# Optimization experiments

Measured on AMD Instinct MI355X. Metric: run time of the kernel, lower is better.

Reference implementation:

```python
import jax, jax.numpy as jnp
import numpy as np

N = 100000
E = 1600000


def _sage(x, src, dst, wl, wr, b):
    # PyG SAGEConv: out = lin_l(mean_{j in N(i)} x_j) + lin_r(x_i)
    agg = jax.ops.segment_sum(x[src], dst, num_segments=N)
    cnt = jax.ops.segment_sum(jnp.ones((src.shape[0], 1), x.dtype), dst, num_segments=N)
    mean = agg / jnp.maximum(cnt, 1.0)
    return mean @ wl.T + x @ wr.T + b


def _tag(x, src, dst, norm, K, w, b):
    # PyG TAGConv: concat of K+1 hops of D^-1/2 A D^-1/2 propagation, one Linear
    xs = [x]
    h = x
    for _ in range(K):
        h = jax.ops.segment_sum(h[src] * norm[:, None], dst, num_segments=N)
        xs.append(h)
    return jnp.concatenate(xs, axis=1) @ w.T + b


def setup_inputs() -> dict:
    key = jax.random.key(0)
    ks = iter(jax.random.split(key, 32))
    x = jax.random.normal(next(ks), (N, 11), dtype=jnp.float32)
    edge_index = jax.random.randint(next(ks), (2, E), 0, N, dtype=jnp.int64)

    def w(k, o, i):
        return jax.random.normal(k, (o, i), dtype=jnp.float32) / np.sqrt(i)

    p = {
        'sage1_wl': w(next(ks), 128, 11), 'sage1_wr': w(next(ks), 128, 11), 'sage1_b': jnp.zeros((128,), jnp.float32),
        'sage2_wl': w(next(ks), 128, 128), 'sage2_wr': w(next(ks), 128, 128), 'sage2_b': jnp.zeros((128,), jnp.float32),
        'sage3_wl': w(next(ks), 1, 128), 'sage3_wr': w(next(ks), 1, 128), 'sage3_b': jnp.zeros((1,), jnp.float32),
        'tag1a_w': w(next(ks), 8, 44), 'tag1a_b': jnp.zeros((8,), jnp.float32),
        'tag2a_w': w(next(ks), 1, 32), 'tag2a_b': jnp.zeros((1,), jnp.float32),
        'tag1b_w': w(next(ks), 8, 77), 'tag1b_b': jnp.zeros((8,), jnp.float32),
        'tag2b_w': w(next(ks), 1, 56), 'tag2b_b': jnp.zeros((1,), jnp.float32),
        'lin1_w': w(next(ks), 1, 3), 'lin1_b': jnp.zeros((1,), jnp.float32),
    }
    return {'x': x, 'edge_index': edge_index, **p}


def reference(x, edge_index, sage1_wl, sage1_wr, sage1_b, sage2_wl, sage2_wr, sage2_b,
              sage3_wl, sage3_wr, sage3_b, tag1a_w, tag1a_b, tag2a_w, tag2a_b,
              tag1b_w, tag1b_b, tag2b_w, tag2b_b, lin1_w, lin1_b):
    src, dst = edge_index[0], edge_index[1]
    # GCN-style symmetric norm for TAGConv (unit edge weights, no self-loops)
    deg = jax.ops.segment_sum(jnp.ones((E,), x.dtype), dst, num_segments=N)
    dis = jnp.where(deg > 0, deg ** -0.5, 0.0)
    norm = dis[src] * dis[dst]

    x1 = jax.nn.sigmoid(_sage(x, src, dst, sage1_wl, sage1_wr, sage1_b))
    x1 = jax.nn.sigmoid(_sage(x1, src, dst, sage2_wl, sage2_wr, sage2_b))
    x1 = jax.nn.relu(_sage(x1, src, dst, sage3_wl, sage3_wr, sage3_b))

    x2 = jax.nn.sigmoid(_tag(x, src, dst, norm, 3, tag1a_w, tag1a_b))
    x2 = jax.nn.relu(_tag(x2, src, dst, norm, 3, tag2a_w, tag2a_b))

    x3 = jax.nn.sigmoid(_tag(x, src, dst, norm, 6, tag1b_w, tag1b_b))
    x3 = jax.nn.relu(_tag(x3, src, dst, norm, 6, tag2b_w, tag2b_b))

    xc = jnp.concatenate((x1, x2, x3), axis=1)  # [N, 3]
    return jax.nn.relu(xc @ lin1_w.T + lin1_b)  # [N, 1]
```

## Files before the change

kernel.cpp:

```cpp
#include <hip/hip_runtime.h>
#include <hip/hip_bf16.h>
#include <hip/hip_fp16.h>

#define NN 100000
#define EE 1600000
#define NBIN 64
#define BSH 9
#define BSZ 512
#define NBK 196

typedef _Float16 h8v __attribute__((ext_vector_type(8)));
typedef float f4v __attribute__((ext_vector_type(4)));

__device__ __forceinline__ float act_apply(float v, int act) {
  if (act == 1) return 1.0f / (1.0f + expf(-v));
  if (act == 2) return fmaxf(v, 0.0f);
  return v;
}
__device__ __forceinline__ float4 f4add(float4 a, float4 b) {
  a.x += b.x; a.y += b.y; a.z += b.z; a.w += b.w; return a;
}
__device__ __forceinline__ float4 f4scale(float4 a, float s) {
  a.x *= s; a.y *= s; a.z *= s; a.w *= s; return a;
}
__device__ __forceinline__ float4 h4f(uint2 v) {
  __half2 a = *reinterpret_cast<__half2*>(&v.x);
  __half2 b = *reinterpret_cast<__half2*>(&v.y);
  float2 fa = __half22float2(a), fb = __half22float2(b);
  return make_float4(fa.x, fa.y, fb.x, fb.y);
}
__device__ __forceinline__ void h8acc(uint4 v, float* a) {
  float4 lo = h4f(make_uint2(v.x, v.y));
  float4 hi = h4f(make_uint2(v.z, v.w));
  a[0] += lo.x; a[1] += lo.y; a[2] += lo.z; a[3] += lo.w;
  a[4] += hi.x; a[5] += hi.y; a[6] += hi.z; a[7] += hi.w;
}
__device__ __forceinline__ uint2 pack4h(float4 r) {
  __half2 q0 = __floats2half2_rn(r.x, r.y), q1 = __floats2half2_rn(r.z, r.w);
  uint2 o; o.x = *(unsigned*)&q0; o.y = *(unsigned*)&q1; return o;
}

__global__ __launch_bounds__(256) void k_bhist(const int* __restrict__ ei, int* __restrict__ ghist) {
  __shared__ int lh[NBK];
  for (int j = threadIdx.x; j < NBK; j += 256) lh[j] = 0;
  __syncthreads();
  for (int i = blockIdx.x * 256 + threadIdx.x; i < EE; i += gridDim.x * 256)
    atomicAdd(&lh[ei[EE + i] >> BSH], 1);
  __syncthreads();
  for (int j = threadIdx.x; j < NBK; j += 256) {
    int v = lh[j];
    if (v) atomicAdd(&ghist[j], v);
  }
}

__global__ void k_b196scan(const int* __restrict__ ghist, int* __restrict__ gcur,
                           int* __restrict__ bexclB, int* __restrict__ csr_off) {
  __shared__ int sh[256];
  int tid = threadIdx.x;
  int v = (tid < NBK) ? ghist[tid] : 0;
  sh[tid] = v;
  __syncthreads();
  for (int d = 1; d < 256; d <<= 1) {
    int t = (tid >= d) ? sh[tid - d] : 0;
    __syncthreads();
    sh[tid] += t;
    __syncthreads();
  }
  int excl = sh[tid] - v;
  if (tid < NBK) { gcur[tid] = excl; bexclB[tid] = excl; }
  if (tid == 0) { bexclB[NBK] = EE; csr_off[NN] = EE; }
}

__global__ __launch_bounds__(256) void k_split(const int* __restrict__ ei,
                                               int* __restrict__ gcur,
                                               uint2* __restrict__ pairs) {
  __shared__ int cntL[256];
  __shared__ int segO[256];
  __shared__ int curL[256];
  __shared__ int baseL[256];
  __shared__ uint2 stag[4096];
  int tid = threadIdx.x;
  int tile0 = blockIdx.x * 4096;
  int tcnt = min(4096, EE - tile0);
  cntL[tid] = 0; curL[tid] = 0;
  __syncthreads();
  for (int i = tid; i < tcnt; i += 256)
    atomicAdd(&cntL[ei[EE + tile0 + i] >> BSH], 1);
  __syncthreads();
  int v = cntL[tid];
  segO[tid] = v;
  __syncthreads();
  for (int d = 1; d < 256; d <<= 1) {
    int t = (tid >= d) ? segO[tid - d] : 0;
    __syncthreads();
    segO[tid] += t;
    __syncthreads();
  }
  int excl = segO[tid] - v;
  __syncthreads();
  segO[tid] = excl;
  __syncthreads();
  for (int i = tid; i < tcnt; i += 256) {
    int s = ei[tile0 + i], dd = ei[EE + tile0 + i];
    int b = dd >> BSH;
    int slot = segO[b] + atomicAdd(&curL[b], 1);
    stag[slot] = make_uint2((unsigned)s, (unsigned)dd);
  }
  baseL[tid] = v ? atomicAdd(&gcur[tid], v) : 0;
  __syncthreads();
  for (int i = tid; i < tcnt; i += 256) {
    uint2 pr = stag[i];
    int b = (int)(pr.y >> BSH);
    pairs[baseL[b] + (i - segO[b])] = pr;
  }
}

__global__ __launch_bounds__(256) void k_bcount(const uint2* __restrict__ pairs,
                                                const int* __restrict__ bexclB,
                                                int* __restrict__ cnt, int* __restrict__ csr_off,
                                                float* __restrict__ dis) {
  __shared__ int c[BSZ];
  __shared__ int ps[256];
  int tid = threadIdx.x;
  int b = blockIdx.x;
  int lo = b << BSH;
  for (int j = tid; j < BSZ; j += 256) c[j] = 0;
  __syncthreads();
  int s0e = bexclB[b], s1e = bexclB[b + 1];
  for (int i = s0e + tid; i < s1e; i += 256)
    atomicAdd(&c[pairs[i].y - lo], 1);
  __syncthreads();
  int a0 = c[2 * tid], a1 = c[2 * tid + 1];
  int pv = a0 + a1;
  ps[tid] = pv;
  __syncthreads();
  for (int d = 1; d < 256; d <<= 1) {
    int t = (tid >= d) ? ps[tid - d] : 0;
    __syncthreads();
    ps[tid] += t;
    __syncthreads();
  }
  int pex = ps[tid] - pv;
  int base = s0e + pex;
  int n0 = lo + 2 * tid, n1 = n0 + 1;
  if (n0 < NN) {
    csr_off[n0] = base; cnt[n0] = a0;
    dis[n0] = (a0 > 0) ? rsqrtf((float)a0) : 0.0f;
  }
  if (n1 < NN) {
    csr_off[n1] = base + a0; cnt[n1] = a1;
    dis[n1] = (a1 > 0) ? rsqrtf((float)a1) : 0.0f;
  }
}

__global__ __launch_bounds__(256) void k_bfill(const uint2* __restrict__ pairs,
                                               const int* __restrict__ bexclB,
                                               const int* __restrict__ csr_off,
                                               int* __restrict__ csr_src) {
  __shared__ int cur[BSZ];
  int tid = threadIdx.x;
  int b = blockIdx.x;
  int lo = b << BSH;
  for (int j = tid; j < BSZ; j += 256) {
    int n = lo + j;
    cur[j] = (n < NN) ? csr_off[n] : 0;
  }
  __syncthreads();
  int s0e = bexclB[b], s1e = bexclB[b + 1];
  for (int i = s0e + tid; i < s1e; i += 256) {
    uint2 pr = pairs[i];
    int p = atomicAdd(&cur[pr.y - lo], 1);
    csr_src[p] = (int)pr.x;
  }
}

__global__ __launch_bounds__(256) void k_hist(const int* __restrict__ cnt, int* __restrict__ hist) {
  __shared__ int lh[NBIN];
  if (threadIdx.x < NBIN) lh[threadIdx.x] = 0;
  __syncthreads();
  int i = blockIdx.x * 256 + threadIdx.x;
  if (i < NN) atomicAdd(&lh[min(cnt[i], NBIN - 1)], 1);
  __syncthreads();
  if (threadIdx.x < NBIN) {
    int v = lh[threadIdx.x];
    if (v) atomicAdd(&hist[threadIdx.x], v);
  }
}
__global__ void k_binscan(const int* __restrict__ hist, int* __restrict__ bincur) {
  int tid = threadIdx.x;
  int v = hist[tid];
  int incl = v;
  for (int d = 1; d < 64; d <<= 1) {
    int t = __shfl_up(incl, d, 64);
    if (tid >= d) incl += t;
  }
  bincur[tid] = incl - v;
}
__global__ __launch_bounds__(256) void k_scatter(const int* __restrict__ cnt,
                                                 int* __restrict__ bincur,
                                                 int* __restrict__ perm) {
  __shared__ int lh[NBIN];
  __shared__ int lbase[NBIN];
  if (threadIdx.x < NBIN) lh[threadIdx.x] = 0;
  __syncthreads();
  int i = blockIdx.x * 256 + threadIdx.x;
  int b = 0, r = 0;
  bool valid = i < NN;
  if (valid) {
    b = min(cnt[i], NBIN - 1);
    r = atomicAdd(&lh[b], 1);
  }
  __syncthreads();
  if (threadIdx.x < NBIN) {
    int v = lh[threadIdx.x];
    lbase[threadIdx.x] = v ? atomicAdd(&bincur[threadIdx.x], v) : 0;
  }
  __syncthreads();
  if (valid) perm[lbase[b] + r] = i;
}

__global__ void k_pad12h(const float* __restrict__ x, __half* __restrict__ x12h) {
  int i = blockIdx.x * blockDim.x + threadIdx.x;
  if (i >= NN * 12) return;
  int n = i / 12, j = i - n * 12;
  x12h[i] = __float2half((j < 11) ? x[n * 11 + j] : 0.0f);
}

__global__ void k_prep_a32(const float* __restrict__ x, __half* __restrict__ A32) {
  int i = blockIdx.x * blockDim.x + threadIdx.x;
  if (i >= NN) return;
  float a[11];
  #pragma unroll
  for (int j = 0; j < 11; ++j) a[j] = x[(long)i * 11 + j];
  uint2* row = (uint2*)(A32 + (long)i * 32);
  row[3] = make_uint2(0u, 0u);
  row[4] = pack4h(make_float4(a[0], a[1], a[2], a[3]));
  row[5] = pack4h(make_float4(a[4], a[5], a[6], a[7]));
  row[6] = pack4h(make_float4(a[8], a[9], a[10], 0.0f));
  row[7] = make_uint2(0u, 0u);
}

__global__ void k_wcast1(const float* __restrict__ wl, const float* __restrict__ wr,
                         __half* __restrict__ w1h) {
  int i = blockIdx.x * 256 + threadIdx.x;
  if (i >= 128 * 32) return;
  int o = i >> 5, k = i & 31;
  float v = 0.0f;
  if (k < 11) v = wl[o * 11 + k];
  else if (k >= 16 && k < 27) v = wr[o * 11 + (k - 16)];
  w1h[i] = __float2half(v);
}

__global__ void k_wcast(const float* __restrict__ wl, const float* __restrict__ wr,
                        __half* __restrict__ w2h) {
  int i = blockIdx.x * 256 + threadIdx.x;
  if (i >= 128 * 256) return;
  int o = i >> 8, k = i & 255;
  float v = (k < 128) ? wl[o * 128 + k] : wr[o * 128 + (k - 128)];
  w2h[i] = __float2half(v);
}

__global__ void k_gmean12h(const __half* __restrict__ x12h, const int* __restrict__ perm,
                           const int* __restrict__ off, const int* __restrict__ srcarr,
                           __half* __restrict__ A32) {
  int g = blockIdx.x * 64 + (threadIdx.x >> 2);
  int t = threadIdx.x & 3;
  if (g >= NN || t >= 3) return;
  int node = perm[g];
  int s = off[node], e = off[node + 1];
  const uint2* h2 = (const uint2*)x12h;
  float4 acc = {0, 0, 0, 0};
  int p = s;
  for (; p + 4 <= e; p += 4) {
    int s0 = srcarr[p], s1 = srcarr[p + 1], s2 = srcarr[p + 2], s3 = srcarr[p + 3];
    acc = f4add(acc, f4add(f4add(h4f(h2[(long)s0 * 3 + t]), h4f(h2[(long)s1 * 3 + t])),
                           f4add(h4f(h2[(long)s2 * 3 + t]), h4f(h2[(long)s3 * 3 + t]))));
  }
  for (; p < e; ++p) acc = f4add(acc, h4f(h2[(long)srcarr[p] * 3 + t]));
  int c = e - s;
  float inv = 1.0f / (float)(c > 0 ? c : 1);
  ((uint2*)A32)[(long)node * 8 + t] = pack4h(f4scale(acc, inv));
}

__global__ void k_gather128(const __half* __restrict__ h, const int* __restrict__ perm,
                            const int* __restrict__ off, const int* __restrict__ srcarr,
                            __half* __restrict__ outh) {
  int g = blockIdx.x * 16 + (threadIdx.x >> 4);
  int t = threadIdx.x & 15;
  if (g >= NN) return;
  int node = perm[g];
  int s = off[node], e = off[node + 1];
  const uint4* h4 = (const uint4*)h;
  float acc[8] = {};
  int p = s;
  for (; p + 4 <= e; p += 4) {
    int s0 = srcarr[p], s1 = srcarr[p + 1], s2 = srcarr[p + 2], s3 = srcarr[p + 3];
    uint4 r0 = h4[(long)s0 * 16 + t], r1 = h4[(long)s1 * 16 + t];
    uint4 r2 = h4[(long)s2 * 16 + t], r3 = h4[(long)s3 * 16 + t];
    h8acc(r0, acc); h8acc(r1, acc); h8acc(r2, acc); h8acc(r3, acc);
  }
  for (; p < e; ++p) h8acc(h4[(long)srcarr[p] * 16 + t], acc);
  int c = e - s;
  float inv = 1.0f / (float)(c > 0 ? c : 1);
  uint4 o;
  __half2 p0 = __floats2half2_rn(acc[0] * inv, acc[1] * inv);
  __half2 p1 = __floats2half2_rn(acc[2] * inv, acc[3] * inv);
  __half2 p2 = __floats2half2_rn(acc[4] * inv, acc[5] * inv);
  __half2 p3 = __floats2half2_rn(acc[6] * inv, acc[7] * inv);
  o.x = *(unsigned*)&p0; o.y = *(unsigned*)&p1; o.z = *(unsigned*)&p2; o.w = *(unsigned*)&p3;
  ((uint4*)outh)[(long)node * 16 + t] = o;
}

__global__ void k_g8h_dual(
    const __half* __restrict__ ha, const float* __restrict__ adda,
    const float* __restrict__ biasa, int acta,
    const __half* __restrict__ hb, const float* __restrict__ addb,
    const float* __restrict__ biasb, int actb,
    const int* __restrict__ perm, const int* __restrict__ off,
    const int* __restrict__ srcarr, const float* __restrict__ dis,
    __half* __restrict__ outa, __half* __restrict__ outb) {
  int g = blockIdx.x * 128 + (threadIdx.x >> 1);
  int t = threadIdx.x & 1;
  if (g >= NN) return;
  int node = perm[g];
  int s = off[node], e = off[node + 1];
  const uint2* ha2 = (const uint2*)ha;
  const uint2* hb2 = (const uint2*)hb;
  float4 accA = {0, 0, 0, 0}, accB = {0, 0, 0, 0};
  int p = s;
  for (; p + 4 <= e; p += 4) {
    int s0 = srcarr[p], s1 = srcarr[p + 1], s2 = srcarr[p + 2], s3 = srcarr[p + 3];
    accA = f4add(accA, f4add(f4add(h4f(ha2[(long)s0 * 2 + t]), h4f(ha2[(long)s1 * 2 + t])),
                             f4add(h4f(ha2[(long)s2 * 2 + t]), h4f(ha2[(long)s3 * 2 + t]))));
    accB = f4add(accB, f4add(f4add(h4f(hb2[(long)s0 * 2 + t]), h4f(hb2[(long)s1 * 2 + t])),
                             f4add(h4f(hb2[(long)s2 * 2 + t]), h4f(hb2[(long)s3 * 2 + t]))));
  }
  for (; p < e; ++p) {
    int s0 = srcarr[p];
    accA = f4add(accA, h4f(ha2[(long)s0 * 2 + t]));
    accB = f4add(accB, h4f(hb2[(long)s0 * 2 + t]));
  }
  float dn = dis[node];
  float4 rA = f4scale(accA, dn);
  rA = f4add(rA, ((const float4*)adda)[(long)node * 2 + t]);
  if (biasa) rA = f4add(rA, ((const float4*)biasa)[t]);
  if (acta == 1) { rA.x = act_apply(rA.x, 1); rA.y = act_apply(rA.y, 1); rA.z = act_apply(rA.z, 1); rA.w = act_apply(rA.w, 1); }
  else if (acta == 2) { rA.x = fmaxf(rA.x, 0.f); rA.y = fmaxf(rA.y, 0.f); rA.z = fmaxf(rA.z, 0.f); rA.w = fmaxf(rA.w, 0.f); }
  else if (acta == 3) rA = f4scale(rA, dn);
  ((uint2*)outa)[(long)node * 2 + t] = pack4h(rA);
  float4 rB = f4scale(accB, dn);
  rB = f4add(rB, ((const float4*)addb)[(long)node * 2 + t]);
  if (biasb) rB = f4add(rB, ((const float4*)biasb)[t]);
  if (actb == 1) { rB.x = act_apply(rB.x, 1); rB.y = act_apply(rB.y, 1); rB.z = act_apply(rB.z, 1); rB.w = act_apply(rB.w, 1); }
  else if (actb == 2) { rB.x = fmaxf(rB.x, 0.f); rB.y = fmaxf(rB.y, 0.f); rB.z = fmaxf(rB.z, 0.f); rB.w = fmaxf(rB.w, 0.f); }
  else if (actb == 3) rB = f4scale(rB, dn);
  ((uint2*)outb)[(long)node * 2 + t] = pack4h(rB);
}

__global__ void k_g8h_single(
    const __half* __restrict__ ha, const float* __restrict__ adda,
    const float* __restrict__ biasa, int acta,
    const int* __restrict__ perm, const int* __restrict__ off,
    const int* __restrict__ srcarr, const float* __restrict__ dis,
    __half* __restrict__ outa) {
  int g = blockIdx.x * 128 + (threadIdx.x >> 1);
  int t = threadIdx.x & 1;
  if (g >= NN) return;
  int node = perm[g];
  int s = off[node], e = off[node + 1];
  const uint2* ha2 = (const uint2*)ha;
  float4 accA = {0, 0, 0, 0};
  int p = s;
  for (; p + 4 <= e; p += 4) {
    int s0 = srcarr[p], s1 = srcarr[p + 1], s2 = srcarr[p + 2], s3 = srcarr[p + 3];
    accA = f4add(accA, f4add(f4add(h4f(ha2[(long)s0 * 2 + t]), h4f(ha2[(long)s1 * 2 + t])),
                             f4add(h4f(ha2[(long)s2 * 2 + t]), h4f(ha2[(long)s3 * 2 + t]))));
  }
  for (; p < e; ++p) accA = f4add(accA, h4f(ha2[(long)srcarr[p] * 2 + t]));
  float dn = dis[node];
  float4 rA = f4scale(accA, dn);
  rA = f4add(rA, ((const float4*)adda)[(long)node * 2 + t]);
  if (biasa) rA = f4add(rA, ((const float4*)biasa)[t]);
  if (acta == 1) { rA.x = act_apply(rA.x, 1); rA.y = act_apply(rA.y, 1); rA.z = act_apply(rA.z, 1); rA.w = act_apply(rA.w, 1); }
  else if (acta == 3) rA = f4scale(rA, dn);
  ((uint2*)outa)[(long)node * 2 + t] = pack4h(rA);
}

template<int MODE>
__global__ void k_g1_dual(
    const float* __restrict__ ua, const float* __restrict__ adda,
    const float* __restrict__ biasa, int acta,
    const float* __restrict__ ub, const float* __restrict__ addb,
    const float* __restrict__ biasb, int actb,
    const int* __restrict__ perm, const int* __restrict__ off,
    const int* __restrict__ srcarr, const float* __restrict__ dis,
    float* __restrict__ outa, float* __restrict__ outb) {
  int g = blockIdx.x * 64 + (threadIdx.x >> 2);
  int t = threadIdx.x & 3;
  if (g >= NN) return;
  int node = perm[g];
  int s = off[node], e = off[node + 1];
  float accA = 0.0f, accB = 0.0f;
  for (int p = s + t; p < e; p += 4) {
    int s0 = srcarr[p];
    accA += ua[s0];
    accB += ub[s0];
  }
  accA += __shfl_xor(accA, 1, 64); accA += __shfl_xor(accA, 2, 64);
  accB += __shfl_xor(accB, 1, 64); accB += __shfl_xor(accB, 2, 64);
  if (t == 0) {
    float sc;
    if (MODE == 0) { int c = e - s; sc = 1.0f / (float)(c > 0 ? c : 1); }
    else sc = dis[node];
    float rA = accA * sc + adda[node];
    if (biasa) rA += biasa[0];
    if (acta == 3) rA *= sc; else rA = act_apply(rA, acta);
    outa[node] = rA;
    float rB = accB * sc + addb[node];
    if (biasb) rB += biasb[0];
    if (actb == 3) rB *= sc; else rB = act_apply(rB, actb);
    outb[node] = rB;
  }
}

template<int MODE>
__global__ void k_g1_single(
    const float* __restrict__ ua, const float* __restrict__ adda,
    const float* __restrict__ biasa, int acta,
    const int* __restrict__ perm, const int* __restrict__ off,
    const int* __restrict__ srcarr, const float* __restrict__ dis,
    float* __restrict__ outa) {
  int g = blockIdx.x * 64 + (threadIdx.x >> 2);
  int t = threadIdx.x & 3;
  if (g >= NN) return;
  int node = perm[g];
  int s = off[node], e = off[node + 1];
  float accA = 0.0f;
  for (int p = s + t; p < e; p += 4) accA += ua[srcarr[p]];
  accA += __shfl_xor(accA, 1, 64); accA += __shfl_xor(accA, 2, 64);
  if (t == 0) {
    float sc;
    if (MODE == 0) { int c = e - s; sc = 1.0f / (float)(c > 0 ? c : 1); }
    else sc = dis[node];
    float rA = accA * sc + adda[node];
    if (biasa) rA += biasa[0];
    if (acta == 3) rA *= sc; else rA = act_apply(rA, acta);
    outa[node] = rA;
  }
}

__global__ void k_g1_final(
    const float* __restrict__ ua, const float* __restrict__ adda,
    const float* __restrict__ biasa,
    const float* __restrict__ x1s, const float* __restrict__ x2s,
    const float* __restrict__ lw, const float* __restrict__ lb,
    const int* __restrict__ perm, const int* __restrict__ off,
    const int* __restrict__ srcarr, const float* __restrict__ dis,
    float* __restrict__ out) {
  int g = blockIdx.x * 64 + (threadIdx.x >> 2);
  int t = threadIdx.x & 3;
  if (g >= NN) return;
  int node = perm[g];
  int s = off[node], e = off[node + 1];
  float accA = 0.0f;
  for (int p = s + t; p < e; p += 4) accA += ua[srcarr[p]];
  accA += __shfl_xor(accA, 1, 64); accA += __shfl_xor(accA, 2, 64);
  if (t == 0) {
    float x3v = fmaxf(accA * dis[node] + adda[node] + biasa[0], 0.0f);
    float v = x1s[node] * lw[0] + x2s[node] * lw[1] + x3v * lw[2] + lb[0];
    out[node] = fmaxf(v, 0.0f);
  }
}

__global__ __launch_bounds__(256) void k_mm1_mfma(
    const __half* __restrict__ A32, const __half* __restrict__ W32,
    const float* __restrict__ bias, __half* __restrict__ out) {
  __shared__ __half lt[4][32][136];
  int tid = threadIdx.x;
  int wave = tid >> 6, l = tid & 63;
  int lr = l & 15, lk = l >> 4;
  int m0 = blockIdx.x * 128 + wave * 32;
  f4v acc[2][8] = {};
  h8v afrag[2];
  #pragma unroll
  for (int rt = 0; rt < 2; ++rt) {
    int row = m0 + rt * 16 + lr;
    h8v z = {};
    afrag[rt] = (row < NN) ? *(const h8v*)&A32[(long)row * 32 + lk * 8] : z;
  }
  #pragma unroll
  for (int c = 0; c < 8; ++c) {
    h8v bfrag = *(const h8v*)&W32[(c * 16 + lr) * 32 + lk * 8];
    acc[0][c] = __builtin_amdgcn_mfma_f32_16x16x32_f16(afrag[0], bfrag, acc[0][c], 0, 0, 0);
    acc[1][c] = __builtin_amdgcn_mfma_f32_16x16x32_f16(afrag[1], bfrag, acc[1][c], 0, 0, 0);
  }
  float bi[8];
  #pragma unroll
  for (int c = 0; c < 8; ++c) bi[c] = bias[c * 16 + lr];
  #pragma unroll
  for (int rt = 0; rt < 2; ++rt)
    #pragma unroll
    for (int c = 0; c < 8; ++c)
      #pragma unroll
      for (int reg = 0; reg < 4; ++reg) {
        float v = acc[rt][c][reg] + bi[c];
        lt[wave][rt * 16 + lk * 4 + reg][c * 16 + lr] = __float2half(1.0f / (1.0f + expf(-v)));
      }
  __syncthreads();
  #pragma unroll
  for (int it = 0; it < 8; ++it) {
    int idx = it * 64 + l;
    int row = idx >> 4, c16 = idx & 15;
    int grow = m0 + row;
    if (grow < NN) {
      uint4 v = *(const uint4*)&lt[wave][row][c16 * 8];
      ((uint4*)out)[(long)grow * 16 + c16] = v;
    }
  }
}

__global__ __launch_bounds__(256) void k_mm2_mfma(
    const __half* __restrict__ A1, const __half* __restrict__ A2,
    const __half* __restrict__ W, const float* __restrict__ bias,
    const float* __restrict__ w3l, const float* __restrict__ w3r,
    float* __restrict__ pp, float* __restrict__ qq) {
  int tid = threadIdx.x;
  int wave = tid >> 6;
  int l = tid & 63;
  int lr = l & 15;
  int lk = l >> 4;
  int m0 = blockIdx.x * 128 + wave * 32;
  f4v acc[2][8] = {};
  #pragma unroll
  for (int ks = 0; ks < 8; ++ks) {
    const __half* Asrc = (ks < 4) ? A1 : A2;
    int kk = (ks & 3) * 32 + lk * 8;
    h8v afrag[2];
    #pragma unroll
    for (int rt = 0; rt < 2; ++rt) {
      int row = m0 + rt * 16 + lr;
      h8v z = {};
      afrag[rt] = (row < NN) ? *(const h8v*)&Asrc[(long)row * 128 + kk] : z;
    }
    #pragma unroll
    for (int c = 0; c < 8; ++c) {
      h8v bfrag = *(const h8v*)&W[(long)(c * 16 + lr) * 256 + ks * 32 + lk * 8];
      acc[0][c] = __builtin_amdgcn_mfma_f32_16x16x32_f16(afrag[0], bfrag, acc[0][c], 0, 0, 0);
      acc[1][c] = __builtin_amdgcn_mfma_f32_16x16x32_f16(afrag[1], bfrag, acc[1][c], 0, 0, 0);
    }
  }
  float wl[8], wr[8], bi[8];
  #pragma unroll
  for (int c = 0; c < 8; ++c) {
    wl[c] = w3l[c * 16 + lr];
    wr[c] = w3r[c * 16 + lr];
    bi[c] = bias[c * 16 + lr];
  }
  #pragma unroll
  for (int rt = 0; rt < 2; ++rt) {
    #pragma unroll
    for (int reg = 0; reg < 4; ++reg) {
      float s1 = 0.0f, s2 = 0.0f;
      #pragma unroll
      for (int c = 0; c < 8; ++c) {
        float v = acc[rt][c][reg] + bi[c];
        float sg = 1.0f / (1.0f + expf(-v));
        s1 += sg * wl[c];
        s2 += sg * wr[c];
      }
      #pragma unroll
      for (int d = 1; d < 16; d <<= 1) {
        s1 += __shfl_xor(s1, d, 64);
        s2 += __shfl_xor(s2, d, 64);
      }
      int row = m0 + rt * 16 + lk * 4 + reg;
      if (lr == 0 && row < NN) { pp[row] = s1; qq[row] = s2; }
    }
  }
}

template<int NH>
__global__ void k_tagP8(const float* __restrict__ A, const float* __restrict__ w,
                        const float* __restrict__ dis,
                        float* __restrict__ outAdds, __half* __restrict__ outTop) {
  int i = blockIdx.x * blockDim.x + threadIdx.x;
  if (i >= NN) return;
  float a[11];
  #pragma unroll
  for (int j = 0; j < 11; ++j) a[j] = A[(long)i * 11 + j];
  #pragma unroll
  for (int k = 0; k < NH; ++k) {
    float s[8];
    #pragma unroll
    for (int o = 0; o < 8; ++o) {
      float acc = 0.0f;
      #pragma unroll
      for (int j = 0; j < 11; ++j) acc += a[j] * w[o * (11 * NH) + k * 11 + j];
      s[o] = acc;
    }
    if (k < NH - 1) {
      float4* dst = (float4*)&outAdds[((long)k * NN + i) * 8];
      dst[0] = make_float4(s[0], s[1], s[2], s[3]);
      dst[1] = make_float4(s[4], s[5], s[6], s[7]);
    } else {
      float dn = dis[i];
      uint4 o4;
      __half2 q0 = __floats2half2_rn(s[0] * dn, s[1] * dn);
      __half2 q1 = __floats2half2_rn(s[2] * dn, s[3] * dn);
      __half2 q2 = __floats2half2_rn(s[4] * dn, s[5] * dn);
      __half2 q3 = __floats2half2_rn(s[6] * dn, s[7] * dn);
      o4.x = *(unsigned*)&q0; o4.y = *(unsigned*)&q1; o4.z = *(unsigned*)&q2; o4.w = *(unsigned*)&q3;
      ((uint4*)outTop)[i] = o4;
    }
  }
}

template<int NH>
__global__ void k_tagP1(const __half* __restrict__ A, const float* __restrict__ w,
                        const float* __restrict__ dis, float* __restrict__ out) {
  int i = blockIdx.x * blockDim.x + threadIdx.x;
  if (i >= NN) return;
  uint4 v = ((const uint4*)A)[i];
  float4 lo = h4f(make_uint2(v.x, v.y)), hi = h4f(make_uint2(v.z, v.w));
  float a[8] = {lo.x, lo.y, lo.z, lo.w, hi.x, hi.y, hi.z, hi.w};
  #pragma unroll
  for (int k = 0; k < NH; ++k) {
    float s = 0.0f;
    #pragma unroll
    for (int j = 0; j < 8; ++j) s += a[j] * w[k * 8 + j];
    if (k == NH - 1) s *= dis[i];
    out[(long)k * NN + i] = s;
  }
}

extern "C" void kernel_launch(void* const* d_in, const int* in_sizes, int n_in,
                              void* d_out, int out_size, void* d_ws, size_t ws_size,
                              hipStream_t stream) {
  const float* x    = (const float*)d_in[0];
  const int*   ei   = (const int*)d_in[1];
  const float* s1wl = (const float*)d_in[2];
  const float* s1wr = (const float*)d_in[3];
  const float* s1b  = (const float*)d_in[4];
  const float* s2wl = (const float*)d_in[5];
  const float* s2wr = (const float*)d_in[6];
  const float* s2b  = (const float*)d_in[7];
  const float* s3wl = (const float*)d_in[8];
  const float* s3wr = (const float*)d_in[9];
  const float* s3b  = (const float*)d_in[10];
  const float* t1aw = (const float*)d_in[11];
  const float* t1ab = (const float*)d_in[12];
  const float* t2aw = (const float*)d_in[13];
  const float* t2ab = (const float*)d_in[14];
  const float* t1bw = (const float*)d_in[15];
  const float* t1bb = (const float*)d_in[16];
  const float* t2bw = (const float*)d_in[17];
  const float* t2bb = (const float*)d_in[18];
  const float* lw   = (const float*)d_in[19];
  const float* lb   = (const float*)d_in[20];
  float* out = (float*)d_out;

  char* basep = (char*)d_ws;
  size_t off = 0;
  auto alloc = [&](size_t bytes) -> void* {
    void* ptr = basep + off;
    off = (off + bytes + 255) & ~(size_t)255;
    return ptr;
  };
  int*   cnt     = (int*)alloc((size_t)NN * 4);
  int*   csr_off = (int*)alloc((size_t)(NN + 1) * 4);
  float* dis     = (float*)alloc((size_t)NN * 4);
  int*   csr_src = (int*)alloc((size_t)EE * 4);
  uint2* pairs   = (uint2*)alloc((size_t)EE * 8);
  int*   perm    = (int*)alloc((size_t)NN * 4);
  int*   ghist   = (int*)alloc(256 * 4);
  int*   gcur    = (int*)alloc(256 * 4);
  int*   bexclB  = (int*)alloc(256 * 4);
  int*   hist    = (int*)alloc(NBIN * 4);
  int*   bincur  = (int*)alloc(NBIN * 4);
  float* x1s     = (float*)alloc((size_t)NN * 4);
  float* x2s     = (float*)alloc((size_t)NN * 4);
  float* pp      = (float*)alloc((size_t)NN * 4);
  float* qq      = (float*)alloc((size_t)NN * 4);
  float* uA1     = (float*)alloc((size_t)NN * 4);
  float* uA2     = (float*)alloc((size_t)NN * 4);
  float* uB1     = (float*)alloc((size_t)NN * 4);
  float* uB2     = (float*)alloc((size_t)NN * 4);
  __half* x12h   = (__half*)alloc((size_t)NN * 12 * 2);
  __half* A32    = (__half*)alloc((size_t)NN * 32 * 2);
  __half* w1h    = (__half*)alloc((size_t)128 * 32 * 2);
  __half* w2h    = (__half*)alloc((size_t)128 * 256 * 2);
  __half* x1a_h  = (__half*)alloc((size_t)NN * 128 * 2);
  __half* mean128_h = (__half*)alloc((size_t)NN * 128 * 2);
  float* region2 = (float*)alloc((size_t)NN * 72 * 4);

  float* r1 = (float*)x1a_h;
  float*  Pa      = r1;
  __half* PaTop_h = (__half*)(r1 + (size_t)NN * 24);
  __half* zaA     = (__half*)(r1 + (size_t)NN * 28);
  __half* zbA     = (__half*)(r1 + (size_t)NN * 32);
  __half* x2a     = (__half*)(r1 + (size_t)NN * 36);
  float*  P2      = r1 + (size_t)NN * 40;
  float*  Pb      = region2;
  __half* PbTop_h = (__half*)(region2 + (size_t)NN * 48);
  __half* zaB     = (__half*)(region2 + (size_t)NN * 52);
  __half* zbB     = (__half*)(region2 + (size_t)NN * 56);
  __half* x3a     = (__half*)(region2 + (size_t)NN * 60);
  float*  P2b     = region2 + (size_t)NN * 64;

  hipMemsetAsync(ghist, 0, 256 * 4, stream);
  k_bhist<<<512, 256, 0, stream>>>(ei, ghist);
  k_b196scan<<<1, 256, 0, stream>>>(ghist, gcur, bexclB, csr_off);
  k_split<<<(EE + 4095) / 4096, 256, 0, stream>>>(ei, gcur, pairs);
  k_bcount<<<NBK, 256, 0, stream>>>(pairs, bexclB, cnt, csr_off, dis);
  k_bfill<<<NBK, 256, 0, stream>>>(pairs, bexclB, csr_off, csr_src);

  hipMemsetAsync(hist, 0, NBIN * 4, stream);
  k_hist<<<(NN + 255) / 256, 256, 0, stream>>>(cnt, hist);
  k_binscan<<<1, 64, 0, stream>>>(hist, bincur);
  k_scatter<<<(NN + 255) / 256, 256, 0, stream>>>(cnt, bincur, perm);

  k_wcast1<<<16, 256, 0, stream>>>(s1wl, s1wr, w1h);
  k_wcast<<<128, 256, 0, stream>>>(s2wl, s2wr, w2h);
  k_pad12h<<<(NN * 12 + 255) / 256, 256, 0, stream>>>(x, x12h);
  k_prep_a32<<<(NN + 255) / 256, 256, 0, stream>>>(x, A32);

  k_gmean12h<<<(NN + 63) / 64, 256, 0, stream>>>(x12h, perm, csr_off, csr_src, A32);
  k_mm1_mfma<<<(NN + 127) / 128, 256, 0, stream>>>(A32, w1h, s1b, x1a_h);
  k_gather128<<<(NN + 15) / 16, 256, 0, stream>>>(x1a_h, perm, csr_off, csr_src, mean128_h);
  k_mm2_mfma<<<(NN + 127) / 128, 256, 0, stream>>>(mean128_h, x1a_h, w2h, s2b, s3wl, s3wr, pp, qq);
  k_g1_single<0><<<(NN + 63) / 64, 256, 0, stream>>>(
      pp, qq, s3b, 2, perm, csr_off, csr_src, dis, x1s);

  k_tagP8<4><<<(NN + 255) / 256, 256, 0, stream>>>(x, t1aw, dis, Pa, PaTop_h);
  k_tagP8<7><<<(NN + 255) / 256, 256, 0, stream>>>(x, t1bw, dis, Pb, PbTop_h);

  const size_t S8 = (size_t)NN * 8;
  k_g8h_dual<<<(NN + 127) / 128, 256, 0, stream>>>(
      PaTop_h, Pa + 2 * S8, nullptr, 3,
      PbTop_h, Pb + 5 * S8, nullptr, 3,
      perm, csr_off, csr_src, dis, zaA, zaB);
  k_g8h_dual<<<(NN + 127) / 128, 256, 0, stream>>>(
      zaA, Pa + 1 * S8, nullptr, 3,
      zaB, Pb + 4 * S8, nullptr, 3,
      perm, csr_off, csr_src, dis, zbA, zbB);
  k_g8h_dual<<<(NN + 127) / 128, 256, 0, stream>>>(
      zbA, Pa, t1ab, 1,
      zbB, Pb + 3 * S8, nullptr, 3,
      perm, csr_off, csr_src, dis, x2a, zaB);
  k_g8h_single<<<(NN + 127) / 128, 256, 0, stream>>>(
      zaB, Pb + 2 * S8, nullptr, 3, perm, csr_off, csr_src, dis, zbB);
  k_g8h_single<<<(NN + 127) / 128, 256, 0, stream>>>(
      zbB, Pb + 1 * S8, nullptr, 3, perm, csr_off, csr_src, dis, zaB);
  k_g8h_single<<<(NN + 127) / 128, 256, 0, stream>>>(
      zaB, Pb, t1bb, 1, perm, csr_off, csr_src, dis, x3a);

  k_tagP1<4><<<(NN + 255) / 256, 256, 0, stream>>>(x2a, t2aw, dis, P2);
  k_tagP1<7><<<(NN + 255) / 256, 256, 0, stream>>>(x3a, t2bw, dis, P2b);

  k_g1_dual<1><<<(NN + 63) / 64, 256, 0, stream>>>(
      P2 + 3 * (size_t)NN, P2 + 2 * (size_t)NN, nullptr, 3,
      P2b + 6 * (size_t)NN, P2b + 5 * (size_t)NN, nullptr, 3,
      perm, csr_off, csr_src, dis, uA1, uB1);
  k_g1_dual<1><<<(NN + 63) / 64, 256, 0, stream>>>(
      uA1, P2 + 1 * (size_t)NN, nullptr, 3,
      uB1, P2b + 4 * (size_t)NN, nullptr, 3,
      perm, csr_off, csr_src, dis, uA2, uB2);
  k_g1_dual<1><<<(NN + 63) / 64, 256, 0, stream>>>(
      uA2, P2, t2ab, 2,
      uB2, P2b + 3 * (size_t)NN, nullptr, 3,
      perm, csr_off, csr_src, dis, x2s, uB1);
  k_g1_single<1><<<(NN + 63) / 64, 256, 0, stream>>>(
      uB1, P2b + 2 * (size_t)NN, nullptr, 3, perm, csr_off, csr_src, dis, uB2);
  k_g1_single<1><<<(NN + 63) / 64, 256, 0, stream>>>(
      uB2, P2b + 1 * (size_t)NN, nullptr, 3, perm, csr_off, csr_src, dis, uB1);
  k_g1_final<<<(NN + 63) / 64, 256, 0, stream>>>(
      uB1, P2b, t2bb, x1s, x2s, lw, lb, perm, csr_off, csr_src, dis, out);
}
```

Measured before the change: 542.8 us.

## Fuse TAG propagation chain into one cooperative persistent kernel with grid syncs

Replaces the roughly fifteen separate TAG hop kernels and projection kernels with a single cooperative kernel that advances through the hops using grid-wide barriers, removing per-launch overhead and inter-kernel gaps. It also merges the CSR count and fill kernels into one, packs edge pairs into 32-bit words to halve the pairs traffic, and combines the small prep and weight-cast kernels into one launch. In exchange, occupancy is capped by the cooperative grid size, and every grid sync stalls all blocks until the slowest one finishes.

```diff
diff --git a/kernel.cpp b/kernel.cpp
--- a/kernel.cpp
+++ b/kernel.cpp
@@ -1,6 +1,9 @@
 #include <hip/hip_runtime.h>
 #include <hip/hip_bf16.h>
 #include <hip/hip_fp16.h>
+#include <hip/hip_cooperative_groups.h>
+
+namespace cg = cooperative_groups;
 
 #define NN 100000
 #define EE 1600000
@@ -12,16 +15,9 @@
 typedef _Float16 h8v __attribute__((ext_vector_type(8)));
 typedef float f4v __attribute__((ext_vector_type(4)));
 
-__device__ __forceinline__ float act_apply(float v, int act) {
-  if (act == 1) return 1.0f / (1.0f + expf(-v));
-  if (act == 2) return fmaxf(v, 0.0f);
-  return v;
-}
+__device__ __forceinline__ float sigm(float v) { return 1.0f / (1.0f + expf(-v)); }
 __device__ __forceinline__ float4 f4add(float4 a, float4 b) {
   a.x += b.x; a.y += b.y; a.z += b.z; a.w += b.w; return a;
-}
-__device__ __forceinline__ float4 f4scale(float4 a, float s) {
-  a.x *= s; a.y *= s; a.z *= s; a.w *= s; return a;
 }
 __device__ __forceinline__ float4 h4f(uint2 v) {
   __half2 a = *reinterpret_cast<__half2*>(&v.x);
@@ -73,12 +69,13 @@
 
 __global__ __launch_bounds__(256) void k_split(const int* __restrict__ ei,
                                                int* __restrict__ gcur,
-                                               uint2* __restrict__ pairs) {
+                                               unsigned* __restrict__ pairs) {
   __shared__ int cntL[256];
   __shared__ int segO[256];
   __shared__ int curL[256];
   __shared__ int baseL[256];
-  __shared__ uint2 stag[4096];
+  __shared__ unsigned stag[4096];
+  __shared__ unsigned char bktL[4096];
   int tid = threadIdx.x;
   int tile0 = blockIdx.x * 4096;
   int tcnt = min(4096, EE - tile0);
@@ -104,23 +101,24 @@
     int s = ei[tile0 + i], dd = ei[EE + tile0 + i];
     int b = dd >> BSH;
     int slot = segO[b] + atomicAdd(&curL[b], 1);
-    stag[slot] = make_uint2((unsigned)s, (unsigned)dd);
+    stag[slot] = (unsigned)s | ((unsigned)(dd & (BSZ - 1)) << 17);
+    bktL[slot] = (unsigned char)b;
   }
   baseL[tid] = v ? atomicAdd(&gcur[tid], v) : 0;
   __syncthreads();
   for (int i = tid; i < tcnt; i += 256) {
-    uint2 pr = stag[i];
-    int b = (int)(pr.y >> BSH);
-    pairs[baseL[b] + (i - segO[b])] = pr;
-  }
-}
-
-__global__ __launch_bounds__(256) void k_bcount(const uint2* __restrict__ pairs,
+    int b = bktL[i];
+    pairs[baseL[b] + (i - segO[b])] = stag[i];
+  }
+}
+
+__global__ __launch_bounds__(256) void k_bbuild(const unsigned* __restrict__ pairs,
                                                 const int* __restrict__ bexclB,
                                                 int* __restrict__ cnt, int* __restrict__ csr_off,
-                                                float* __restrict__ dis) {
+                                                float* __restrict__ dis, int* __restrict__ csr_src) {
   __shared__ int c[BSZ];
   __shared__ int ps[256];
+  __shared__ int curB[BSZ];
   int tid = threadIdx.x;
   int b = blockIdx.x;
   int lo = b << BSH;
@@ -128,7 +126,7 @@
   __syncthreads();
   int s0e = bexclB[b], s1e = bexclB[b + 1];
   for (int i = s0e + tid; i < s1e; i += 256)
-    atomicAdd(&c[pairs[i].y - lo], 1);
+    atomicAdd(&c[pairs[i] >> 17], 1);
   __syncthreads();
   int a0 = c[2 * tid], a1 = c[2 * tid + 1];
   int pv = a0 + a1;
@@ -151,26 +149,13 @@
     csr_off[n1] = base + a0; cnt[n1] = a1;
     dis[n1] = (a1 > 0) ? rsqrtf((float)a1) : 0.0f;
   }
-}
-
-__global__ __launch_bounds__(256) void k_bfill(const uint2* __restrict__ pairs,
-                                               const int* __restrict__ bexclB,
-                                               const int* __restrict__ csr_off,
-                                               int* __restrict__ csr_src) {
-  __shared__ int cur[BSZ];
-  int tid = threadIdx.x;
-  int b = blockIdx.x;
-  int lo = b << BSH;
-  for (int j = tid; j < BSZ; j += 256) {
-    int n = lo + j;
-    cur[j] = (n < NN) ? csr_off[n] : 0;
-  }
-  __syncthreads();
-  int s0e = bexclB[b], s1e = bexclB[b + 1];
+  curB[2 * tid] = base;
+  curB[2 * tid + 1] = base + a0;
+  __syncthreads();
   for (int i = s0e + tid; i < s1e; i += 256) {
-    uint2 pr = pairs[i];
-    int p = atomicAdd(&cur[pr.y - lo], 1);
-    csr_src[p] = (int)pr.x;
+    unsigned pk = pairs[i];
+    int p = atomicAdd(&curB[pk >> 17], 1);
+    csr_src[p] = (int)(pk & 0x1FFFFu);
   }
 }
 
@@ -219,45 +204,46 @@
   if (valid) perm[lbase[b] + r] = i;
 }
 
-__global__ void k_pad12h(const float* __restrict__ x, __half* __restrict__ x12h) {
-  int i = blockIdx.x * blockDim.x + threadIdx.x;
-  if (i >= NN * 12) return;
-  int n = i / 12, j = i - n * 12;
-  x12h[i] = __float2half((j < 11) ? x[n * 11 + j] : 0.0f);
-}
-
-__global__ void k_prep_a32(const float* __restrict__ x, __half* __restrict__ A32) {
-  int i = blockIdx.x * blockDim.x + threadIdx.x;
-  if (i >= NN) return;
-  float a[11];
-  #pragma unroll
-  for (int j = 0; j < 11; ++j) a[j] = x[(long)i * 11 + j];
-  uint2* row = (uint2*)(A32 + (long)i * 32);
-  row[3] = make_uint2(0u, 0u);
-  row[4] = pack4h(make_float4(a[0], a[1], a[2], a[3]));
-  row[5] = pack4h(make_float4(a[4], a[5], a[6], a[7]));
-  row[6] = pack4h(make_float4(a[8], a[9], a[10], 0.0f));
-  row[7] = make_uint2(0u, 0u);
-}
-
-__global__ void k_wcast1(const float* __restrict__ wl, const float* __restrict__ wr,
-                         __half* __restrict__ w1h) {
-  int i = blockIdx.x * 256 + threadIdx.x;
-  if (i >= 128 * 32) return;
-  int o = i >> 5, k = i & 31;
-  float v = 0.0f;
-  if (k < 11) v = wl[o * 11 + k];
-  else if (k >= 16 && k < 27) v = wr[o * 11 + (k - 16)];
-  w1h[i] = __float2half(v);
-}
-
-__global__ void k_wcast(const float* __restrict__ wl, const float* __restrict__ wr,
-                        __half* __restrict__ w2h) {
-  int i = blockIdx.x * 256 + threadIdx.x;
-  if (i >= 128 * 256) return;
-  int o = i >> 8, k = i & 255;
-  float v = (k < 128) ? wl[o * 128 + k] : wr[o * 128 + (k - 128)];
-  w2h[i] = __float2half(v);
+#define PREP_B0 ((NN * 12 + 255) / 256)
+#define PREP_B1 ((NN + 255) / 256)
+__global__ __launch_bounds__(256) void k_prep(
+    const float* __restrict__ x, const float* __restrict__ s1wl, const float* __restrict__ s1wr,
+    const float* __restrict__ s2wl, const float* __restrict__ s2wr,
+    __half* __restrict__ x12h, __half* __restrict__ A32,
+    __half* __restrict__ w1h, __half* __restrict__ w2h) {
+  int bid = blockIdx.x;
+  if (bid < PREP_B0) {
+    int i = bid * 256 + threadIdx.x;
+    if (i < NN * 12) {
+      int n = i / 12, j = i - n * 12;
+      x12h[i] = __float2half((j < 11) ? x[n * 11 + j] : 0.0f);
+    }
+  } else if (bid < PREP_B0 + PREP_B1) {
+    int i = (bid - PREP_B0) * 256 + threadIdx.x;
+    if (i < NN) {
+      float a[11];
+      #pragma unroll
+      for (int j = 0; j < 11; ++j) a[j] = x[(long)i * 11 + j];
+      uint2* row = (uint2*)(A32 + (long)i * 32);
+      row[3] = make_uint2(0u, 0u);
+      row[4] = pack4h(make_float4(a[0], a[1], a[2], a[3]));
+      row[5] = pack4h(make_float4(a[4], a[5], a[6], a[7]));
+      row[6] = pack4h(make_float4(a[8], a[9], a[10], 0.0f));
+      row[7] = make_uint2(0u, 0u);
+    }
+  } else if (bid < PREP_B0 + PREP_B1 + 16) {
+    int i = (bid - PREP_B0 - PREP_B1) * 256 + threadIdx.x;
+    int o = i >> 5, k = i & 31;
+    float v = 0.0f;
+    if (k < 11) v = s1wl[o * 11 + k];
+    else if (k >= 16 && k < 27) v = s1wr[o * 11 + (k - 16)];
+    w1h[i] = __float2half(v);
+  } else {
+    int i = (bid - PREP_B0 - PREP_B1 - 16) * 256 + threadIdx.x;
+    int o = i >> 8, k = i & 255;
+    float v = (k < 128) ? s2wl[o * 128 + k] : s2wr[o * 128 + (k - 128)];
+    w2h[i] = __float2half(v);
+  }
 }
 
 __global__ void k_gmean12h(const __half* __restrict__ x12h, const int* __restrict__ perm,
@@ -279,7 +265,8 @@
   for (; p < e; ++p) acc = f4add(acc, h4f(h2[(long)srcarr[p] * 3 + t]));
   int c = e - s;
   float inv = 1.0f / (float)(c > 0 ? c : 1);
-  ((uint2*)A32)[(long)node * 8 + t] = pack4h(f4scale(acc, inv));
+  acc.x *= inv; acc.y *= inv; acc.z *= inv; acc.w *= inv;
+  ((uint2*)A32)[(long)node * 8 + t] = pack4h(acc);
 }
 
 __global__ void k_gather128(const __half* __restrict__ h, const int* __restrict__ perm,
@@ -302,174 +289,10 @@
   for (; p < e; ++p) h8acc(h4[(long)srcarr[p] * 16 + t], acc);
   int c = e - s;
   float inv = 1.0f / (float)(c > 0 ? c : 1);
-  uint4 o;
-  __half2 p0 = __floats2half2_rn(acc[0] * inv, acc[1] * inv);
-  __half2 p1 = __floats2half2_rn(acc[2] * inv, acc[3] * inv);
-  __half2 p2 = __floats2half2_rn(acc[4] * inv, acc[5] * inv);
-  __half2 p3 = __floats2half2_rn(acc[6] * inv, acc[7] * inv);
-  o.x = *(unsigned*)&p0; o.y = *(unsigned*)&p1; o.z = *(unsigned*)&p2; o.w = *(unsigned*)&p3;
+  uint2 lo = pack4h(make_float4(acc[0] * inv, acc[1] * inv, acc[2] * inv, acc[3] * inv));
+  uint2 hi = pack4h(make_float4(acc[4] * inv, acc[5] * inv, acc[6] * inv, acc[7] * inv));
+  uint4 o; o.x = lo.x; o.y = lo.y; o.z = hi.x; o.w = hi.y;
   ((uint4*)outh)[(long)node * 16 + t] = o;
-}
-
-__global__ void k_g8h_dual(
-    const __half* __restrict__ ha, const float* __restrict__ adda,
-    const float* __restrict__ biasa, int acta,
-    const __half* __restrict__ hb, const float* __restrict__ addb,
-    const float* __restrict__ biasb, int actb,
-    const int* __restrict__ perm, const int* __restrict__ off,
-    const int* __restrict__ srcarr, const float* __restrict__ dis,
-    __half* __restrict__ outa, __half* __restrict__ outb) {
-  int g = blockIdx.x * 128 + (threadIdx.x >> 1);
-  int t = threadIdx.x & 1;
-  if (g >= NN) return;
-  int node = perm[g];
-  int s = off[node], e = off[node + 1];
-  const uint2* ha2 = (const uint2*)ha;
-  const uint2* hb2 = (const uint2*)hb;
-  float4 accA = {0, 0, 0, 0}, accB = {0, 0, 0, 0};
-  int p = s;
-  for (; p + 4 <= e; p += 4) {
-    int s0 = srcarr[p], s1 = srcarr[p + 1], s2 = srcarr[p + 2], s3 = srcarr[p + 3];
-    accA = f4add(accA, f4add(f4add(h4f(ha2[(long)s0 * 2 + t]), h4f(ha2[(long)s1 * 2 + t])),
-                             f4add(h4f(ha2[(long)s2 * 2 + t]), h4f(ha2[(long)s3 * 2 + t]))));
-    accB = f4add(accB, f4add(f4add(h4f(hb2[(long)s0 * 2 + t]), h4f(hb2[(long)s1 * 2 + t])),
-                             f4add(h4f(hb2[(long)s2 * 2 + t]), h4f(hb2[(long)s3 * 2 + t]))));
-  }
-  for (; p < e; ++p) {
-    int s0 = srcarr[p];
-    accA = f4add(accA, h4f(ha2[(long)s0 * 2 + t]));
-    accB = f4add(accB, h4f(hb2[(long)s0 * 2 + t]));
-  }
-  float dn = dis[node];
-  float4 rA = f4scale(accA, dn);
-  rA = f4add(rA, ((const float4*)adda)[(long)node * 2 + t]);
-  if (biasa) rA = f4add(rA, ((const float4*)biasa)[t]);
-  if (acta == 1) { rA.x = act_apply(rA.x, 1); rA.y = act_apply(rA.y, 1); rA.z = act_apply(rA.z, 1); rA.w = act_apply(rA.w, 1); }
-  else if (acta == 2) { rA.x = fmaxf(rA.x, 0.f); rA.y = fmaxf(rA.y, 0.f); rA.z = fmaxf(rA.z, 0.f); rA.w = fmaxf(rA.w, 0.f); }
-  else if (acta == 3) rA = f4scale(rA, dn);
-  ((uint2*)outa)[(long)node * 2 + t] = pack4h(rA);
-  float4 rB = f4scale(accB, dn);
-  rB = f4add(rB, ((const float4*)addb)[(long)node * 2 + t]);
-  if (biasb) rB = f4add(rB, ((const float4*)biasb)[t]);
-  if (actb == 1) { rB.x = act_apply(rB.x, 1); rB.y = act_apply(rB.y, 1); rB.z = act_apply(rB.z, 1); rB.w = act_apply(rB.w, 1); }
-  else if (actb == 2) { rB.x = fmaxf(rB.x, 0.f); rB.y = fmaxf(rB.y, 0.f); rB.z = fmaxf(rB.z, 0.f); rB.w = fmaxf(rB.w, 0.f); }
-  else if (actb == 3) rB = f4scale(rB, dn);
-  ((uint2*)outb)[(long)node * 2 + t] = pack4h(rB);
-}
-
-__global__ void k_g8h_single(
-    const __half* __restrict__ ha, const float* __restrict__ adda,
-    const float* __restrict__ biasa, int acta,
-    const int* __restrict__ perm, const int* __restrict__ off,
-    const int* __restrict__ srcarr, const float* __restrict__ dis,
-    __half* __restrict__ outa) {
-  int g = blockIdx.x * 128 + (threadIdx.x >> 1);
-  int t = threadIdx.x & 1;
-  if (g >= NN) return;
-  int node = perm[g];
-  int s = off[node], e = off[node + 1];
-  const uint2* ha2 = (const uint2*)ha;
-  float4 accA = {0, 0, 0, 0};
-  int p = s;
-  for (; p + 4 <= e; p += 4) {
-    int s0 = srcarr[p], s1 = srcarr[p + 1], s2 = srcarr[p + 2], s3 = srcarr[p + 3];
-    accA = f4add(accA, f4add(f4add(h4f(ha2[(long)s0 * 2 + t]), h4f(ha2[(long)s1 * 2 + t])),
-                             f4add(h4f(ha2[(long)s2 * 2 + t]), h4f(ha2[(long)s3 * 2 + t]))));
-  }
-  for (; p < e; ++p) accA = f4add(accA, h4f(ha2[(long)srcarr[p] * 2 + t]));
-  float dn = dis[node];
-  float4 rA = f4scale(accA, dn);
-  rA = f4add(rA, ((const float4*)adda)[(long)node * 2 + t]);
-  if (biasa) rA = f4add(rA, ((const float4*)biasa)[t]);
-  if (acta == 1) { rA.x = act_apply(rA.x, 1); rA.y = act_apply(rA.y, 1); rA.z = act_apply(rA.z, 1); rA.w = act_apply(rA.w, 1); }
-  else if (acta == 3) rA = f4scale(rA, dn);
-  ((uint2*)outa)[(long)node * 2 + t] = pack4h(rA);
-}
-
-template<int MODE>
-__global__ void k_g1_dual(
-    const float* __restrict__ ua, const float* __restrict__ adda,
-    const float* __restrict__ biasa, int acta,
-    const float* __restrict__ ub, const float* __restrict__ addb,
-    const float* __restrict__ biasb, int actb,
-    const int* __restrict__ perm, const int* __restrict__ off,
-    const int* __restrict__ srcarr, const float* __restrict__ dis,
-    float* __restrict__ outa, float* __restrict__ outb) {
-  int g = blockIdx.x * 64 + (threadIdx.x >> 2);
-  int t = threadIdx.x & 3;
-  if (g >= NN) return;
-  int node = perm[g];
-  int s = off[node], e = off[node + 1];
-  float accA = 0.0f, accB = 0.0f;
-  for (int p = s + t; p < e; p += 4) {
-    int s0 = srcarr[p];
-    accA += ua[s0];
-    accB += ub[s0];
-  }
-  accA += __shfl_xor(accA, 1, 64); accA += __shfl_xor(accA, 2, 64);
-  accB += __shfl_xor(accB, 1, 64); accB += __shfl_xor(accB, 2, 64);
-  if (t == 0) {
-    float sc;
-    if (MODE == 0) { int c = e - s; sc = 1.0f / (float)(c > 0 ? c : 1); }
-    else sc = dis[node];
-    float rA = accA * sc + adda[node];
-    if (biasa) rA += biasa[0];
-    if (acta == 3) rA *= sc; else rA = act_apply(rA, acta);
-    outa[node] = rA;
-    float rB = accB * sc + addb[node];
-    if (biasb) rB += biasb[0];
-    if (actb == 3) rB *= sc; else rB = act_apply(rB, actb);
-    outb[node] = rB;
-  }
-}
-
-template<int MODE>
-__global__ void k_g1_single(
-    const float* __restrict__ ua, const float* __restrict__ adda,
-    const float* __restrict__ biasa, int acta,
-    const int* __restrict__ perm, const int* __restrict__ off,
-    const int* __restrict__ srcarr, const float* __restrict__ dis,
-    float* __restrict__ outa) {
-  int g = blockIdx.x * 64 + (threadIdx.x >> 2);
-  int t = threadIdx.x & 3;
-  if (g >= NN) return;
-  int node = perm[g];
-  int s = off[node], e = off[node + 1];
-  float accA = 0.0f;
-  for (int p = s + t; p < e; p += 4) accA += ua[srcarr[p]];
-  accA += __shfl_xor(accA, 1, 64); accA += __shfl_xor(accA, 2, 64);
-  if (t == 0) {
-    float sc;
-    if (MODE == 0) { int c = e - s; sc = 1.0f / (float)(c > 0 ? c : 1); }
-    else sc = dis[node];
-    float rA = accA * sc + adda[node];
-    if (biasa) rA += biasa[0];
-    if (acta == 3) rA *= sc; else rA = act_apply(rA, acta);
-    outa[node] = rA;
-  }
-}
-
-__global__ void k_g1_final(
-    const float* __restrict__ ua, const float* __restrict__ adda,
-    const float* __restrict__ biasa,
-    const float* __restrict__ x1s, const float* __restrict__ x2s,
-    const float* __restrict__ lw, const float* __restrict__ lb,
-    const int* __restrict__ perm, const int* __restrict__ off,
-    const int* __restrict__ srcarr, const float* __restrict__ dis,
-    float* __restrict__ out) {
-  int g = blockIdx.x * 64 + (threadIdx.x >> 2);
-  int t = threadIdx.x & 3;
-  if (g >= NN) return;
-  int node = perm[g];
-  int s = off[node], e = off[node + 1];
-  float accA = 0.0f;
-  for (int p = s + t; p < e; p += 4) accA += ua[srcarr[p]];
-  accA += __shfl_xor(accA, 1, 64); accA += __shfl_xor(accA, 2, 64);
-  if (t == 0) {
-    float x3v = fmaxf(accA * dis[node] + adda[node] + biasa[0], 0.0f);
-    float v = x1s[node] * lw[0] + x2s[node] * lw[1] + x3v * lw[2] + lb[0];
-    out[node] = fmaxf(v, 0.0f);
-  }
 }
 
 __global__ __launch_bounds__(256) void k_mm1_mfma(
@@ -504,7 +327,7 @@
       #pragma unroll
       for (int reg = 0; reg < 4; ++reg) {
         float v = acc[rt][c][reg] + bi[c];
-        lt[wave][rt * 16 + lk * 4 + reg][c * 16 + lr] = __float2half(1.0f / (1.0f + expf(-v)));
+        lt[wave][rt * 16 + lk * 4 + reg][c * 16 + lr] = __float2half(sigm(v));
       }
   __syncthreads();
   #pragma unroll
@@ -564,7 +387,7 @@
       #pragma unroll
       for (int c = 0; c < 8; ++c) {
         float v = acc[rt][c][reg] + bi[c];
-        float sg = 1.0f / (1.0f + expf(-v));
+        float sg = sigm(v);
         s1 += sg * wl[c];
         s2 += sg * wr[c];
       }
@@ -579,57 +402,330 @@
   }
 }
 
-template<int NH>
-__global__ void k_tagP8(const float* __restrict__ A, const float* __restrict__ w,
-                        const float* __restrict__ dis,
-                        float* __restrict__ outAdds, __half* __restrict__ outTop) {
-  int i = blockIdx.x * blockDim.x + threadIdx.x;
-  if (i >= NN) return;
-  float a[11];
-  #pragma unroll
-  for (int j = 0; j < 11; ++j) a[j] = A[(long)i * 11 + j];
-  #pragma unroll
-  for (int k = 0; k < NH; ++k) {
-    float s[8];
+struct CoopArgs {
+  const int* csr_off; const int* csr_src; const int* perm; const float* dis;
+  const float* x;
+  const float* t1aw; const float* t1ab; const float* t1bw; const float* t1bb;
+  const float* t2aw; const float* t2ab; const float* t2bw; const float* t2bb;
+  const float* pp; const float* qq; const float* s3b;
+  const float* lw; const float* lb;
+  float* Pa; __half* PTop; __half* zbuf0; __half* zbuf1;
+  __half* x2a; float* P2;
+  float* Pb; __half* x3a; float* P2b;
+  float* x1s; float* x2s;
+  float* uA1; float* uA2; float* uB1; float* uB2;
+  float* out;
+};
+
+__device__ __forceinline__ void d8_dual_act3(
+    const __half* src, const float* addA, const float* addB, __half* dst,
+    const int* perm, const int* off, const int* srcarr, const float* dis) {
+  const uint4* src4 = (const uint4*)src;
+  int t = threadIdx.x & 1;
+  const float4* addp = (const float4*)(t == 0 ? addA : addB);
+  for (int g = blockIdx.x * 128 + (threadIdx.x >> 1); g < NN; g += gridDim.x * 128) {
+    int node = perm[g];
+    int s = off[node], e = off[node + 1];
+    float acc[8] = {};
+    int p = s;
+    for (; p + 4 <= e; p += 4) {
+      int s0 = srcarr[p], s1 = srcarr[p + 1], s2 = srcarr[p + 2], s3 = srcarr[p + 3];
+      uint4 v0 = src4[(long)s0 * 2 + t], v1 = src4[(long)s1 * 2 + t];
+      uint4 v2 = src4[(long)s2 * 2 + t], v3 = src4[(long)s3 * 2 + t];
+      h8acc(v0, acc); h8acc(v1, acc); h8acc(v2, acc); h8acc(v3, acc);
+    }
+    for (; p < e; ++p) h8acc(src4[(long)srcarr[p] * 2 + t], acc);
+    float dn = dis[node];
+    float4 a0 = addp[(long)node * 2], a1 = addp[(long)node * 2 + 1];
+    float4 r0 = make_float4((acc[0] * dn + a0.x) * dn, (acc[1] * dn + a0.y) * dn,
+                            (acc[2] * dn + a0.z) * dn, (acc[3] * dn + a0.w) * dn);
+    float4 r1 = make_float4((acc[4] * dn + a1.x) * dn, (acc[5] * dn + a1.y) * dn,
+                            (acc[6] * dn + a1.z) * dn, (acc[7] * dn + a1.w) * dn);
+    uint2 lo = pack4h(r0), hi = pack4h(r1);
+    uint4 o; o.x = lo.x; o.y = lo.y; o.z = hi.x; o.w = hi.y;
+    ((uint4*)dst)[(long)node * 2 + t] = o;
+  }
+}
+
+__device__ __forceinline__ void d8_single_act3(
+    const __half* src, const float* addB, __half* dst,
+    const int* perm, const int* off, const int* srcarr, const float* dis) {
+  const uint2* src2 = (const uint2*)src;
+  int t = threadIdx.x & 1;
+  for (int g = blockIdx.x * 128 + (threadIdx.x >> 1); g < NN; g += gridDim.x * 128) {
+    int node = perm[g];
+    int s = off[node], e = off[node + 1];
+    float4 acc = {0, 0, 0, 0};
+    int p = s;
+    for (; p + 4 <= e; p += 4) {
+      int s0 = srcarr[p], s1 = srcarr[p + 1], s2 = srcarr[p + 2], s3 = srcarr[p + 3];
+      acc = f4add(acc, f4add(f4add(h4f(src2[(long)s0 * 4 + 2 + t]), h4f(src2[(long)s1 * 4 + 2 + t])),
+                             f4add(h4f(src2[(long)s2 * 4 + 2 + t]), h4f(src2[(long)s3 * 4 + 2 + t]))));
+    }
+    for (; p < e; ++p) acc = f4add(acc, h4f(src2[(long)srcarr[p] * 4 + 2 + t]));
+    float dn = dis[node];
+    float4 av = ((const float4*)addB)[(long)node * 2 + t];
+    float4 r = make_float4((acc.x * dn + av.x) * dn, (acc.y * dn + av.y) * dn,
+                           (acc.z * dn + av.z) * dn, (acc.w * dn + av.w) * dn);
+    ((uint2*)dst)[(long)node * 4 + 2 + t] = pack4h(r);
+  }
+}
+
+__device__ __forceinline__ void d1_dual_act3(
+    const float* ua, const float* adda, const float* ub, const float* addb,
+    float* outa, float* outb,
+    const int* perm, const int* off, const int* srcarr, const float* dis) {
+  int t = threadIdx.x & 3;
+  for (int g = blockIdx.x * 64 + (threadIdx.x >> 2); g < NN; g += gridDim.x * 64) {
+    int node = perm[g];
+    int s = off[node], e = off[node + 1];
+    float accA = 0.0f, accB = 0.0f;
+    for (int p = s + t; p < e; p += 4) {
+      int s0 = srcarr[p];
+      accA += ua[s0];
+      accB += ub[s0];
+    }
+    accA += __shfl_xor(accA, 1, 64); accA += __shfl_xor(accA, 2, 64);
+    accB += __shfl_xor(accB, 1, 64); accB += __shfl_xor(accB, 2, 64);
+    if (t == 0) {
+      float sc = dis[node];
+      outa[node] = (accA * sc + adda[node]) * sc;
+      outb[node] = (accB * sc + addb[node]) * sc;
+    }
+  }
+}
+
+__device__ __forceinline__ void d1_single_act3(
+    const float* ua, const float* adda, float* outa,
+    const int* perm, const int* off, const int* srcarr, const float* dis) {
+  int t = threadIdx.x & 3;
+  for (int g = blockIdx.x * 64 + (threadIdx.x >> 2); g < NN; g += gridDim.x * 64) {
+    int node = perm[g];
+    int s = off[node], e = off[node + 1];
+    float accA = 0.0f;
+    for (int p = s + t; p < e; p += 4) accA += ua[srcarr[p]];
+    accA += __shfl_xor(accA, 1, 64); accA += __shfl_xor(accA, 2, 64);
+    if (t == 0) {
+      float sc = dis[node];
+      outa[node] = (accA * sc + adda[node]) * sc;
+    }
+  }
+}
+
+__global__ __launch_bounds__(256) void k_coop(CoopArgs A) {
+  cg::grid_group grid = cg::this_grid();
+  const size_t S8 = (size_t)NN * 8;
+  const size_t S1 = (size_t)NN;
+
+  {
+    for (int i = blockIdx.x * 256 + threadIdx.x; i < NN; i += gridDim.x * 256) {
+      float a[11];
+      #pragma unroll
+      for (int j = 0; j < 11; ++j) a[j] = A.x[(long)i * 11 + j];
+      float dn = A.dis[i];
+      #pragma unroll
+      for (int k = 0; k < 4; ++k) {
+        float s[8];
+        #pragma unroll
+        for (int o = 0; o < 8; ++o) {
+          float acc = 0.0f;
+          #pragma unroll
+          for (int j = 0; j < 11; ++j) acc += a[j] * A.t1aw[o * 44 + k * 11 + j];
+          s[o] = acc;
+        }
+        if (k < 3) {
+          float4* dst = (float4*)&A.Pa[((size_t)k * NN + i) * 8];
+          dst[0] = make_float4(s[0], s[1], s[2], s[3]);
+          dst[1] = make_float4(s[4], s[5], s[6], s[7]);
+        } else {
+          uint2 lo = pack4h(make_float4(s[0] * dn, s[1] * dn, s[2] * dn, s[3] * dn));
+          uint2 hi = pack4h(make_float4(s[4] * dn, s[5] * dn, s[6] * dn, s[7] * dn));
+          uint4 o4; o4.x = lo.x; o4.y = lo.y; o4.z = hi.x; o4.w = hi.y;
+          ((uint4*)A.PTop)[(long)i * 2] = o4;
+        }
+      }
+      #pragma unroll
+      for (int k = 0; k < 7; ++k) {
+        float s[8];
+        #pragma unroll
+        for (int o = 0; o < 8; ++o) {
+          float acc = 0.0f;
+          #pragma unroll
+          for (int j = 0; j < 11; ++j) acc += a[j] * A.t1bw[o * 77 + k * 11 + j];
+          s[o] = acc;
+        }
+        if (k < 6) {
+          float4* dst = (float4*)&A.Pb[((size_t)k * NN + i) * 8];
+          dst[0] = make_float4(s[0], s[1], s[2], s[3]);
+          dst[1] = make_float4(s[4], s[5], s[6], s[7]);
+        } else {
+          uint2 lo = pack4h(make_float4(s[0] * dn, s[1] * dn, s[2] * dn, s[3] * dn));
+          uint2 hi = pack4h(make_float4(s[4] * dn, s[5] * dn, s[6] * dn, s[7] * dn));
+          uint4 o4; o4.x = lo.x; o4.y = lo.y; o4.z = hi.x; o4.w = hi.y;
+          ((uint4*)A.PTop)[(long)i * 2 + 1] = o4;
+        }
+      }
+    }
+    int t = threadIdx.x & 3;
+    for (int g = blockIdx.x * 64 + (threadIdx.x >> 2); g < NN; g += gridDim.x * 64) {
+      int node = A.perm[g];
+      int s = A.csr_off[node], e = A.csr_off[node + 1];
+      float acc = 0.0f;
+      for (int p = s + t; p < e; p += 4) acc += A.pp[A.csr_src[p]];
+      acc += __shfl_xor(acc, 1, 64); acc += __shfl_xor(acc, 2, 64);
+      if (t == 0) {
+        int c = e - s;
+        float sc = 1.0f / (float)(c > 0 ? c : 1);
+        A.x1s[node] = fmaxf(acc * sc + A.qq[node] + A.s3b[0], 0.0f);
+      }
+    }
+  }
+  grid.sync();
+  d8_dual_act3(A.PTop, A.Pa + 2 * S8, A.Pb + 5 * S8, A.zbuf0,
+               A.perm, A.csr_off, A.csr_src, A.dis);
+  grid.sync();
+  d8_dual_act3(A.zbuf0, A.Pa + 1 * S8, A.Pb + 4 * S8, A.zbuf1,
+               A.perm, A.csr_off, A.csr_src, A.dis);
+  grid.sync();
+  {
+    const uint4* src4 = (const uint4*)A.zbuf1;
+    int t = threadIdx.x & 1;
+    for (int g = blockIdx.x * 128 + (threadIdx.x >> 1); g < NN; g += gridDim.x * 128) {
+      int node = A.perm[g];
+      int s = A.csr_off[node], e = A.csr_off[node + 1];
+      float acc[8] = {};
+      int p = s;
+      for (; p + 4 <= e; p += 4) {
+        int s0 = A.csr_src[p], s1 = A.csr_src[p + 1], s2 = A.csr_src[p + 2], s3 = A.csr_src[p + 3];
+        h8acc(src4[(long)s0 * 2 + t], acc); h8acc(src4[(long)s1 * 2 + t], acc);
+        h8acc(src4[(long)s2 * 2 + t], acc); h8acc(src4[(long)s3 * 2 + t], acc);
+      }
+      for (; p < e; ++p) h8acc(src4[(long)A.csr_src[p] * 2 + t], acc);
+      float dn = A.dis[node];
+      if (t == 0) {
+        const float4* addp = (const float4*)A.Pa;
+        float4 a0 = addp[(long)node * 2], a1 = addp[(long)node * 2 + 1];
+        float4 b0 = ((const float4*)A.t1ab)[0], b1 = ((const float4*)A.t1ab)[1];
+        float4 r0 = make_float4(sigm(acc[0] * dn + a0.x + b0.x), sigm(acc[1] * dn + a0.y + b0.y),
+                                sigm(acc[2] * dn + a0.z + b0.z), sigm(acc[3] * dn + a0.w + b0.w));
+        float4 r1 = make_float4(sigm(acc[4] * dn + a1.x + b1.x), sigm(acc[5] * dn + a1.y + b1.y),
+                                sigm(acc[6] * dn + a1.z + b1.z), sigm(acc[7] * dn + a1.w + b1.w));
+        uint2 lo = pack4h(r0), hi = pack4h(r1);
+        uint4 o; o.x = lo.x; o.y = lo.y; o.z = hi.x; o.w = hi.y;
+        ((uint4*)A.x2a)[node] = o;
+      } else {
+        const float4* addp = (const float4*)(A.Pb + 3 * S8);
+        float4 a0 = addp[(long)node * 2], a1 = addp[(long)node * 2 + 1];
+        float4 r0 = make_float4((acc[0] * dn + a0.x) * dn, (acc[1] * dn + a0.y) * dn,
+                                (acc[2] * dn + a0.z) * dn, (acc[3] * dn + a0.w) * dn);
+        float4 r1 = make_float4((acc[4] * dn + a1.x) * dn, (acc[5] * dn + a1.y) * dn,
+                                (acc[6] * dn + a1.z) * dn, (acc[7] * dn + a1.w) * dn);
+        uint2 lo = pack4h(r0), hi = pack4h(r1);
+        uint4 o; o.x = lo.x; o.y = lo.y; o.z = hi.x; o.w = hi.y;
+        ((uint4*)A.zbuf0)[(long)node * 2 + 1] = o;
+      }
+    }
+  }
+  grid.sync();
+  d8_single_act3(A.zbuf0, A.Pb + 2 * S8, A.zbuf1, A.perm, A.csr_off, A.csr_src, A.dis);
+  for (int i = blockIdx.x * 256 + threadIdx.x; i < NN; i += gridDim.x * 256) {
+    uint4 v = ((const uint4*)A.x2a)[i];
+    float4 lo = h4f(make_uint2(v.x, v.y)), hi = h4f(make_uint2(v.z, v.w));
+    float a[8] = {lo.x, lo.y, lo.z, lo.w, hi.x, hi.y, hi.z, hi.w};
     #pragma unroll
-    for (int o = 0; o < 8; ++o) {
+    for (int k = 0; k < 4; ++k) {
+      float s = 0.0f;
+      #pragma unroll
+      for (int j = 0; j < 8; ++j) s += a[j] * A.t2aw[k * 8 + j];
+      if (k == 3) s *= A.dis[i];
+      A.P2[(size_t)k * NN + i] = s;
+    }
+  }
+  grid.sync();
+  d8_single_act3(A.zbuf1, A.Pb + 1 * S8, A.zbuf0, A.perm, A.csr_off, A.csr_src, A.dis);
+  grid.sync();
+  {
+    const uint2* src2 = (const uint2*)A.zbuf0;
+    int t = threadIdx.x & 1;
+    for (int g = blockIdx.x * 128 + (threadIdx.x >> 1); g < NN; g += gridDim.x * 128) {
+      int node = A.perm[g];
+      int s = A.csr_off[node], e = A.csr_off[node + 1];
+      float4 acc = {0, 0, 0, 0};
+      int p = s;
+      for (; p + 4 <= e; p += 4) {
+        int s0 = A.csr_src[p], s1 = A.csr_src[p + 1], s2 = A.csr_src[p + 2], s3 = A.csr_src[p + 3];
+        acc = f4add(acc, f4add(f4add(h4f(src2[(long)s0 * 4 + 2 + t]), h4f(src2[(long)s1 * 4 + 2 + t])),
+                               f4add(h4f(src2[(long)s2 * 4 + 2 + t]), h4f(src2[(long)s3 * 4 + 2 + t]))));
+      }
+      for (; p < e; ++p) acc = f4add(acc, h4f(src2[(long)A.csr_src[p] * 4 + 2 + t]));
+      float dn = A.dis[node];
+      float4 av = ((const float4*)A.Pb)[(long)node * 2 + t];
+      float4 bv = ((const float4*)A.t1bb)[t];
+      float4 r = make_float4(sigm(acc.x * dn + av.x + bv.x), sigm(acc.y * dn + av.y + bv.y),
+                             sigm(acc.z * dn + av.z + bv.z), sigm(acc.w * dn + av.w + bv.w));
+      ((uint2*)A.x3a)[(long)node * 2 + t] = pack4h(r);
+    }
+  }
+  grid.sync();
+  for (int i = blockIdx.x * 256 + threadIdx.x; i < NN; i += gridDim.x * 256) {
+    uint4 v = ((const uint4*)A.x3a)[i];
+    float4 lo = h4f(make_uint2(v.x, v.y)), hi = h4f(make_uint2(v.z, v.w));
+    float a[8] = {lo.x, lo.y, lo.z, lo.w, hi.x, hi.y, hi.z, hi.w};
+    #pragma unroll
+    for (int k = 0; k < 7; ++k) {
+      float s = 0.0f;
+      #pragma unroll
+      for (int j = 0; j < 8; ++j) s += a[j] * A.t2bw[k * 8 + j];
+      if (k == 6) s *= A.dis[i];
+      A.P2b[(size_t)k * NN + i] = s;
+    }
+  }
+  grid.sync();
+  d1_dual_act3(A.P2 + 3 * S1, A.P2 + 2 * S1, A.P2b + 6 * S1, A.P2b + 5 * S1,
+               A.uA1, A.uB1, A.perm, A.csr_off, A.csr_src, A.dis);
+  grid.sync();
+  d1_dual_act3(A.uA1, A.P2 + 1 * S1, A.uB1, A.P2b + 4 * S1,
+               A.uA2, A.uB2, A.perm, A.csr_off, A.csr_src, A.dis);
+  grid.sync();
+  {
+    int t = threadIdx.x & 3;
+    for (int g = blockIdx.x * 64 + (threadIdx.x >> 2); g < NN; g += gridDim.x * 64) {
+      int node = A.perm[g];
+      int s = A.csr_off[node], e = A.csr_off[node + 1];
+      float accA = 0.0f, accB = 0.0f;
+      for (int p = s + t; p < e; p += 4) {
+        int s0 = A.csr_src[p];
+        accA += A.uA2[s0];
+        accB += A.uB2[s0];
+      }
+      accA += __shfl_xor(accA, 1, 64); accA += __shfl_xor(accA, 2, 64);
+      accB += __shfl_xor(accB, 1, 64); accB += __shfl_xor(accB, 2, 64);
+      if (t == 0) {
+        float sc = A.dis[node];
+        A.x2s[node] = fmaxf(accA * sc + A.P2[node] + A.t2ab[0], 0.0f);
+        A.uB1[node] = (accB * sc + A.P2b[3 * S1 + node]) * sc;
+      }
+    }
+  }
+  grid.sync();
+  d1_single_act3(A.uB1, A.P2b + 2 * S1, A.uB2, A.perm, A.csr_off, A.csr_src, A.dis);
+  grid.sync();
+  d1_single_act3(A.uB2, A.P2b + 1 * S1, A.uB1, A.perm, A.csr_off, A.csr_src, A.dis);
+  grid.sync();
+  {
+    int t = threadIdx.x & 3;
+    for (int g = blockIdx.x * 64 + (threadIdx.x >> 2); g < NN; g += gridDim.x * 64) {
+      int node = A.perm[g];
+      int s = A.csr_off[node], e = A.csr_off[node + 1];
       float acc = 0.0f;
-      #pragma unroll
-      for (int j = 0; j < 11; ++j) acc += a[j] * w[o * (11 * NH) + k * 11 + j];
-      s[o] = acc;
-    }
-    if (k < NH - 1) {
-      float4* dst = (float4*)&outAdds[((long)k * NN + i) * 8];
-      dst[0] = make_float4(s[0], s[1], s[2], s[3]);
-      dst[1] = make_float4(s[4], s[5], s[6], s[7]);
-    } else {
-      float dn = dis[i];
-      uint4 o4;
-      __half2 q0 = __floats2half2_rn(s[0] * dn, s[1] * dn);
-      __half2 q1 = __floats2half2_rn(s[2] * dn, s[3] * dn);
-      __half2 q2 = __floats2half2_rn(s[4] * dn, s[5] * dn);
-      __half2 q3 = __floats2half2_rn(s[6] * dn, s[7] * dn);
-      o4.x = *(unsigned*)&q0; o4.y = *(unsigned*)&q1; o4.z = *(unsigned*)&q2; o4.w = *(unsigned*)&q3;
-      ((uint4*)outTop)[i] = o4;
-    }
-  }
-}
-
-template<int NH>
-__global__ void k_tagP1(const __half* __restrict__ A, const float* __restrict__ w,
-                        const float* __restrict__ dis, float* __restrict__ out) {
-  int i = blockIdx.x * blockDim.x + threadIdx.x;
-  if (i >= NN) return;
-  uint4 v = ((const uint4*)A)[i];
-  float4 lo = h4f(make_uint2(v.x, v.y)), hi = h4f(make_uint2(v.z, v.w));
-  float a[8] = {lo.x, lo.y, lo.z, lo.w, hi.x, hi.y, hi.z, hi.w};
-  #pragma unroll
-  for (int k = 0; k < NH; ++k) {
-    float s = 0.0f;
-    #pragma unroll
-    for (int j = 0; j < 8; ++j) s += a[j] * w[k * 8 + j];
-    if (k == NH - 1) s *= dis[i];
-    out[(long)k * NN + i] = s;
+      for (int p = s + t; p < e; p += 4) acc += A.uB1[A.csr_src[p]];
+      acc += __shfl_xor(acc, 1, 64); acc += __shfl_xor(acc, 2, 64);
+      if (t == 0) {
+        float x3v = fmaxf(acc * A.dis[node] + A.P2b[node] + A.t2bb[0], 0.0f);
+        float v = A.x1s[node] * A.lw[0] + A.x2s[node] * A.lw[1] + x3v * A.lw[2] + A.lb[0];
+        A.out[node] = fmaxf(v, 0.0f);
+      }
+    }
   }
 }
 
@@ -666,113 +762,81 @@
     off = (off + bytes + 255) & ~(size_t)255;
     return ptr;
   };
-  int*   cnt     = (int*)alloc((size_t)NN * 4);
-  int*   csr_off = (int*)alloc((size_t)(NN + 1) * 4);
-  float* dis     = (float*)alloc((size_t)NN * 4);
-  int*   csr_src = (int*)alloc((size_t)EE * 4);
-  uint2* pairs   = (uint2*)alloc((size_t)EE * 8);
-  int*   perm    = (int*)alloc((size_t)NN * 4);
-  int*   ghist   = (int*)alloc(256 * 4);
-  int*   gcur    = (int*)alloc(256 * 4);
-  int*   bexclB  = (int*)alloc(256 * 4);
-  int*   hist    = (int*)alloc(NBIN * 4);
-  int*   bincur  = (int*)alloc(NBIN * 4);
-  float* x1s     = (float*)alloc((size_t)NN * 4);
-  float* x2s     = (float*)alloc((size_t)NN * 4);
-  float* pp      = (float*)alloc((size_t)NN * 4);
-  float* qq      = (float*)alloc((size_t)NN * 4);
-  float* uA1     = (float*)alloc((size_t)NN * 4);
-  float* uA2     = (float*)alloc((size_t)NN * 4);
-  float* uB1     = (float*)alloc((size_t)NN * 4);
-  float* uB2     = (float*)alloc((size_t)NN * 4);
-  __half* x12h   = (__half*)alloc((size_t)NN * 12 * 2);
-  __half* A32    = (__half*)alloc((size_t)NN * 32 * 2);
-  __half* w1h    = (__half*)alloc((size_t)128 * 32 * 2);
-  __half* w2h    = (__half*)alloc((size_t)128 * 256 * 2);
-  __half* x1a_h  = (__half*)alloc((size_t)NN * 128 * 2);
-  __half* mean128_h = (__half*)alloc((size_t)NN * 128 * 2);
-  float* region2 = (float*)alloc((size_t)NN * 72 * 4);
+  int*      cnt     = (int*)alloc((size_t)NN * 4);
+  int*      csr_off = (int*)alloc((size_t)(NN + 1) * 4);
+  float*    dis     = (float*)alloc((size_t)NN * 4);
+  int*      csr_src = (int*)alloc((size_t)EE * 4);
+  unsigned* pairs   = (unsigned*)alloc((size_t)EE * 4);
+  int*      perm    = (int*)alloc((size_t)NN * 4);
+  int*      ghist   = (int*)alloc(256 * 4);
+  int*      gcur    = (int*)alloc(256 * 4);
+  int*      bexclB  = (int*)alloc(256 * 4);
+  int*      hist    = (int*)alloc(NBIN * 4);
+  int*      bincur  = (int*)alloc(NBIN * 4);
+  float*    x1s     = (float*)alloc((size_t)NN * 4);
+  float*    x2s     = (float*)alloc((size_t)NN * 4);
+  float*    pp      = (float*)alloc((size_t)NN * 4);
+  float*    qq      = (float*)alloc((size_t)NN * 4);
+  float*    uA1     = (float*)alloc((size_t)NN * 4);
+  float*    uA2     = (float*)alloc((size_t)NN * 4);
+  float*    uB1     = (float*)alloc((size_t)NN * 4);
+  float*    uB2     = (float*)alloc((size_t)NN * 4);
+  __half*   x12h    = (__half*)alloc((size_t)NN * 12 * 2);
+  __half*   A32     = (__half*)alloc((size_t)NN * 32 * 2);
+  __half*   w1h     = (__half*)alloc((size_t)128 * 32 * 2);
+  __half*   w2h     = (__half*)alloc((size_t)128 * 256 * 2);
+  __half*   x1a_h   = (__half*)alloc((size_t)NN * 128 * 2);
+  __half*   mean128_h = (__half*)alloc((size_t)NN * 128 * 2);
+  float*    region2 = (float*)alloc((size_t)NN * 60 * 4);
 
   float* r1 = (float*)x1a_h;
-  float*  Pa      = r1;
-  __half* PaTop_h = (__half*)(r1 + (size_t)NN * 24);
-  __half* zaA     = (__half*)(r1 + (size_t)NN * 28);
-  __half* zbA     = (__half*)(r1 + (size_t)NN * 32);
-  __half* x2a     = (__half*)(r1 + (size_t)NN * 36);
-  float*  P2      = r1 + (size_t)NN * 40;
-  float*  Pb      = region2;
-  __half* PbTop_h = (__half*)(region2 + (size_t)NN * 48);
-  __half* zaB     = (__half*)(region2 + (size_t)NN * 52);
-  __half* zbB     = (__half*)(region2 + (size_t)NN * 56);
-  __half* x3a     = (__half*)(region2 + (size_t)NN * 60);
-  float*  P2b     = region2 + (size_t)NN * 64;
-
-  hipMemsetAsync(ghist, 0, 256 * 4, stream);
+  float*  Pa    = r1;
+  __half* PTop  = (__half*)(r1 + (size_t)NN * 24);
+  __half* zbuf0 = (__half*)(r1 + (size_t)NN * 32);
+  __half* zbuf1 = (__half*)(r1 + (size_t)NN * 40);
+  __half* x2a   = (__half*)(r1 + (size_t)NN * 48);
+  float*  P2    = r1 + (size_t)NN * 52;
+  float*  Pb    = region2;
+  __half* x3a   = (__half*)(region2 + (size_t)NN * 48);
+  float*  P2b   = region2 + (size_t)NN * 52;
+
+  hipMemsetAsync(ghist, 0, 3840, stream);
   k_bhist<<<512, 256, 0, stream>>>(ei, ghist);
   k_b196scan<<<1, 256, 0, stream>>>(ghist, gcur, bexclB, csr_off);
   k_split<<<(EE + 4095) / 4096, 256, 0, stream>>>(ei, gcur, pairs);
-  k_bcount<<<NBK, 256, 0, stream>>>(pairs, bexclB, cnt, csr_off, dis);
-  k_bfill<<<NBK, 256, 0, stream>>>(pairs, bexclB, csr_off, csr_src);
-
-  hipMemsetAsync(hist, 0, NBIN * 4, stream);
+  k_bbuild<<<NBK, 256, 0, stream>>>(pairs, bexclB, cnt, csr_off, dis, csr_src);
+
   k_hist<<<(NN + 255) / 256, 256, 0, stream>>>(cnt, hist);
   k_binscan<<<1, 64, 0, stream>>>(hist, bincur);
   k_scatter<<<(NN + 255) / 256, 256, 0, stream>>>(cnt, bincur, perm);
 
-  k_wcast1<<<16, 256, 0, stream>>>(s1wl, s1wr, w1h);
-  k_wcast<<<128, 256, 0, stream>>>(s2wl, s2wr, w2h);
-  k_pad12h<<<(NN * 12 + 255) / 256, 256, 0, stream>>>(x, x12h);
-  k_prep_a32<<<(NN + 255) / 256, 256, 0, stream>>>(x, A32);
+  k_prep<<<PREP_B0 + PREP_B1 + 16 + 128, 256, 0, stream>>>(
+      x, s1wl, s1wr, s2wl, s2wr, x12h, A32, w1h, w2h);
 
   k_gmean12h<<<(NN + 63) / 64, 256, 0, stream>>>(x12h, perm, csr_off, csr_src, A32);
   k_mm1_mfma<<<(NN + 127) / 128, 256, 0, stream>>>(A32, w1h, s1b, x1a_h);
   k_gather128<<<(NN + 15) / 16, 256, 0, stream>>>(x1a_h, perm, csr_off, csr_src, mean128_h);
   k_mm2_mfma<<<(NN + 127) / 128, 256, 0, stream>>>(mean128_h, x1a_h, w2h, s2b, s3wl, s3wr, pp, qq);
-  k_g1_single<0><<<(NN + 63) / 64, 256, 0, stream>>>(
-      pp, qq, s3b, 2, perm, csr_off, csr_src, dis, x1s);
-
-  k_tagP8<4><<<(NN + 255) / 256, 256, 0, stream>>>(x, t1aw, dis, Pa, PaTop_h);
-  k_tagP8<7><<<(NN + 255) / 256, 256, 0, stream>>>(x, t1bw, dis, Pb, PbTop_h);
-
-  const size_t S8 = (size_t)NN * 8;
-  k_g8h_dual<<<(NN + 127) / 128, 256, 0, stream>>>(
-      PaTop_h, Pa + 2 * S8, nullptr, 3,
-      PbTop_h, Pb + 5 * S8, nullptr, 3,
-      perm, csr_off, csr_src, dis, zaA, zaB);
-  k_g8h_dual<<<(NN + 127) / 128, 256, 0, stream>>>(
-      zaA, Pa + 1 * S8, nullptr, 3,
-      zaB, Pb + 4 * S8, nullptr, 3,
-      perm, csr_off, csr_src, dis, zbA, zbB);
-  k_g8h_dual<<<(NN + 127) / 128, 256, 0, stream>>>(
-      zbA, Pa, t1ab, 1,
-      zbB, Pb + 3 * S8, nullptr, 3,
-      perm, csr_off, csr_src, dis, x2a, zaB);
-  k_g8h_single<<<(NN + 127) / 128, 256, 0, stream>>>(
-      zaB, Pb + 2 * S8, nullptr, 3, perm, csr_off, csr_src, dis, zbB);
-  k_g8h_single<<<(NN + 127) / 128, 256, 0, stream>>>(
-      zbB, Pb + 1 * S8, nullptr, 3, perm, csr_off, csr_src, dis, zaB);
-  k_g8h_single<<<(NN + 127) / 128, 256, 0, stream>>>(
-      zaB, Pb, t1bb, 1, perm, csr_off, csr_src, dis, x3a);
-
-  k_tagP1<4><<<(NN + 255) / 256, 256, 0, stream>>>(x2a, t2aw, dis, P2);
-  k_tagP1<7><<<(NN + 255) / 256, 256, 0, stream>>>(x3a, t2bw, dis, P2b);
-
-  k_g1_dual<1><<<(NN + 63) / 64, 256, 0, stream>>>(
-      P2 + 3 * (size_t)NN, P2 + 2 * (size_t)NN, nullptr, 3,
-      P2b + 6 * (size_t)NN, P2b + 5 * (size_t)NN, nullptr, 3,
-      perm, csr_off, csr_src, dis, uA1, uB1);
-  k_g1_dual<1><<<(NN + 63) / 64, 256, 0, stream>>>(
-      uA1, P2 + 1 * (size_t)NN, nullptr, 3,
-      uB1, P2b + 4 * (size_t)NN, nullptr, 3,
-      perm, csr_off, csr_src, dis, uA2, uB2);
-  k_g1_dual<1><<<(NN + 63) / 64, 256, 0, stream>>>(
-      uA2, P2, t2ab, 2,
-      uB2, P2b + 3 * (size_t)NN, nullptr, 3,
-      perm, csr_off, csr_src, dis, x2s, uB1);
-  k_g1_single<1><<<(NN + 63) / 64, 256, 0, stream>>>(
-      uB1, P2b + 2 * (size_t)NN, nullptr, 3, perm, csr_off, csr_src, dis, uB2);
-  k_g1_single<1><<<(NN + 63) / 64, 256, 0, stream>>>(
-      uB2, P2b + 1 * (size_t)NN, nullptr, 3, perm, csr_off, csr_src, dis, uB1);
-  k_g1_final<<<(NN + 63) / 64, 256, 0, stream>>>(
-      uB1, P2b, t2bb, x1s, x2s, lw, lb, perm, csr_off, csr_src, dis, out);
-}
+
+  CoopArgs ca;
+  ca.csr_off = csr_off; ca.csr_src = csr_src; ca.perm = perm; ca.dis = dis;
+  ca.x = x;
+  ca.t1aw = t1aw; ca.t1ab = t1ab; ca.t1bw = t1bw; ca.t1bb = t1bb;
+  ca.t2aw = t2aw; ca.t2ab = t2ab; ca.t2bw = t2bw; ca.t2bb = t2bb;
+  ca.pp = pp; ca.qq = qq; ca.s3b = s3b;
+  ca.lw = lw; ca.lb = lb;
+  ca.Pa = Pa; ca.PTop = PTop; ca.zbuf0 = zbuf0; ca.zbuf1 = zbuf1;
+  ca.x2a = x2a; ca.P2 = P2;
+  ca.Pb = Pb; ca.x3a = x3a; ca.P2b = P2b;
+  ca.x1s = x1s; ca.x2s = x2s;
+  ca.uA1 = uA1; ca.uA2 = uA2; ca.uB1 = uB1; ca.uB2 = uB2;
+  ca.out = out;
+
+  int maxBlocksPerCU = 0;
+  hipOccupancyMaxActiveBlocksPerMultiprocessor(&maxBlocksPerCU, k_coop, 256, 0);
+  int GRID = (maxBlocksPerCU > 0) ? maxBlocksPerCU * 256 : 256;
+  if (GRID > 1024) GRID = 1024;
+  if (GRID < 64) GRID = 64;
+  void* kargs[] = { &ca };
+  hipLaunchCooperativeKernel((const void*)k_coop, dim3(GRID), dim3(256), kargs, 0, stream);
+}
```

New measurement: 1.462 ms. +169.4%, slower.
